# Performance work log

Hardware: AMD Instinct MI355X
Metric: run time of the kernel (lower is better)

## Reference

```python
import jax, jax.numpy as jnp
import numpy as np

# Irreps structure (hardcoded per init_kwargs):
#  input  = 16x0e + 8x1o  -> dim 16 + 8*3 = 40
#  query  = key = 8x0e + 4x1o -> dim 8 + 4*3 = 20
#  output = 16x0e + 8x1o -> dim 40
#  edge_sh = 1x0e + 1x1o -> dim 4
M0, M1 = 16, 8          # input multiplicities (scalar, vector)
Q0, Q1 = 8, 4           # query/key multiplicities
O0, O1 = 16, 8          # output multiplicities
TPK_NUMEL = M0*Q0 + M1*Q0 + M0*Q1 + M1*Q1 + M1*Q1   # 320
TPV_NUMEL = M0*O0 + M1*O0 + M0*O1 + M1*O1 + M1*O1   # 640
EDGE_BASIS = 16
HIDDEN = 32


def _split(x):
    """Split irreps vector [*, m0 + 3*m1] into scalars [*, m0] and vectors [*, m1, 3]."""
    m0 = x.shape[-1] - 3 * ((x.shape[-1] - M0) // 3) if False else None
    return x  # placeholder, not used


def fc_net(x, w1, w2):
    """e3nn FullyConnectedNet: no biases, 1/sqrt(fan_in) scaling, silu hidden act."""
    h = jax.nn.silu((x @ w1) * (1.0 / np.sqrt(x.shape[-1])))
    return (h @ w2) * (1.0 / np.sqrt(w1.shape[-1]))


def fctp_edge(xs, xv, shs, shv, w, o0, o1):
    """FullyConnectedTensorProduct((m0x0e+m1x1o) x (1x0e+1x1o) -> (o0x0e+o1x1o))
    with per-edge weights w [E, numel]. Component-normalized CG, path-normalized output.
    xs:[E,m0] xv:[E,m1,3] shs:[E,1] shv:[E,3]."""
    m0, m1 = xs.shape[1], xv.shape[1]
    sizes = [m0*o0, m1*o0, m0*o1, m1*o1, m1*o1]
    offs = np.cumsum([0] + sizes)
    w1 = w[:, offs[0]:offs[1]].reshape(-1, m0, o0)
    w2 = w[:, offs[1]:offs[2]].reshape(-1, m1, o0)
    w3 = w[:, offs[2]:offs[3]].reshape(-1, m0, o1)
    w4 = w[:, offs[3]:offs[4]].reshape(-1, m1, o1)
    w5 = w[:, offs[4]:offs[5]].reshape(-1, m1, o1)
    # scalar output paths: 0e x 0e -> 0e ; 1o x 1o -> 0e (dot / sqrt3)
    p_ss = xs * shs                                            # [E,m0]
    p_vv = jnp.einsum('eic,ec->ei', xv, shv) * (1.0/np.sqrt(3.0))  # [E,m1]
    out_s = (jnp.einsum('ei,eio->eo', p_ss, w1)
             + jnp.einsum('ei,eio->eo', p_vv, w2)) * (1.0/np.sqrt(m0 + m1))
    # vector output paths: 0e x 1o ; 1o x 0e ; 1o x 1o -> 1o (cross / sqrt2)
    p_sv = xs[:, :, None] * shv[:, None, :]                    # [E,m0,3]
    p_vs = xv * shs[:, :, None]                                # [E,m1,3]
    p_xx = jnp.cross(xv, shv[:, None, :]) * (1.0/np.sqrt(2.0)) # [E,m1,3]
    out_v = (jnp.einsum('eic,eio->eoc', p_sv, w3)
             + jnp.einsum('eic,eio->eoc', p_vs, w4)
             + jnp.einsum('eic,eio->eoc', p_xx, w5)) * (1.0/np.sqrt(m0 + 2*m1))
    return out_s, out_v


def setup_inputs() -> dict:
    key = jax.random.key(0)
    ks = jax.random.split(key, 12)
    N, E = 10000, 100000
    node_ft = jax.random.normal(ks[0], (N, M0 + 3*M1), dtype=jnp.float32)
    edge_index = jax.random.randint(ks[1], (2, E), 0, N, dtype=jnp.int64)
    edge_sh = jax.random.normal(ks[2], (E, 4), dtype=jnp.float32)
    edge_scalars = jax.random.uniform(ks[3], (E, EDGE_BASIS), dtype=jnp.float32)
    # learned parameters
    w_q_s = jax.random.normal(ks[4], (M0, Q0), dtype=jnp.float32)
    w_q_v = jax.random.normal(ks[5], (M1, Q1), dtype=jnp.float32)
    fck_w1 = jax.random.normal(ks[6], (EDGE_BASIS, HIDDEN), dtype=jnp.float32)
    fck_w2 = jax.random.normal(ks[7], (HIDDEN, TPK_NUMEL), dtype=jnp.float32)
    fcv_w1 = jax.random.normal(ks[8], (EDGE_BASIS, HIDDEN), dtype=jnp.float32)
    fcv_w2 = jax.random.normal(ks[9], (HIDDEN, TPV_NUMEL), dtype=jnp.float32)
    wdot_s = jax.random.normal(ks[10], (Q0, Q0), dtype=jnp.float32)
    wdot_v = jax.random.normal(ks[11], (Q1, Q1), dtype=jnp.float32)
    return dict(node_ft=node_ft, edge_index=edge_index, edge_sh=edge_sh,
                edge_scalars=edge_scalars, w_q_s=w_q_s, w_q_v=w_q_v,
                fck_w1=fck_w1, fck_w2=fck_w2, fcv_w1=fcv_w1, fcv_w2=fcv_w2,
                wdot_s=wdot_s, wdot_v=wdot_v)


def reference(node_ft, edge_index, edge_sh, edge_scalars, w_q_s, w_q_v,
              fck_w1, fck_w2, fcv_w1, fcv_w2, wdot_s, wdot_v):
    N = node_ft.shape[0]
    sender, receiver = edge_index[0], edge_index[1]
    x_s = node_ft[:, :M0]                       # [N,16]
    x_v = node_ft[:, M0:].reshape(N, M1, 3)     # [N,8,3]
    # q = o3.Linear(input -> query): per-irrep linear mixing, 1/sqrt(mul) norm
    q_s = (x_s @ w_q_s) * (1.0/np.sqrt(M0))                    # [N,Q0]
    q_v = jnp.einsum('nic,io->noc', x_v, w_q_v) * (1.0/np.sqrt(M1))  # [N,Q1,3]
    sh_s, sh_v = edge_sh[:, :1], edge_sh[:, 1:4]
    xs_e, xv_e = x_s[sender], x_v[sender]       # gather sender features
    # per-edge tensor-product weights from radial MLPs
    wk = fc_net(edge_scalars, fck_w1, fck_w2)   # [E, 320]
    wv = fc_net(edge_scalars, fcv_w1, fcv_w2)   # [E, 640]
    k_s, k_v = fctp_edge(xs_e, xv_e, sh_s, sh_v, wk, Q0, Q1)
    v_s, v_v = fctp_edge(xs_e, xv_e, sh_s, sh_v, wv, O0, O1)
    # dot = FCTP(query, key -> 0e) with shared internal weights
    qr_s, qr_v = q_s[receiver], q_v[receiver]
    fan = Q0*Q0 + Q1*Q1
    dot = (jnp.einsum('ei,ej,ij->e', qr_s, k_s, wdot_s)
           + jnp.einsum('eic,ejc,ij->e', qr_v, k_v, wdot_v) * (1.0/np.sqrt(3.0))
           ) * (1.0/np.sqrt(fan))               # [E]
    # scatter-softmax over receiver
    ex = jnp.exp(dot)
    z = jax.ops.segment_sum(ex, receiver, num_segments=N)      # [N]
    alpha = ex / z[receiver]
    a = jnp.sqrt(jax.nn.relu(alpha))            # [E]
    out_s = jax.ops.segment_sum(a[:, None] * v_s, receiver, num_segments=N)
    out_v = jax.ops.segment_sum(a[:, None, None] * v_v, receiver, num_segments=N)
    return jnp.concatenate([out_s, out_v.reshape(N, O1*3)], axis=-1)  # [N,40]
```

## Files before the change

### kernel.cpp

```cpp
#include <hip/hip_runtime.h>


#define BS 256
#define EPB 64

typedef _Float16 h2 __attribute__((ext_vector_type(2)));

__device__ __forceinline__ float silu_f(float x) {
    return x * (1.0f / (1.0f + __expf(-x)));
}
__device__ __forceinline__ unsigned short f2h(float f) {
    return __builtin_bit_cast(unsigned short, (_Float16)f);
}
__device__ __forceinline__ unsigned pk2h(float a, float b) {
    return (unsigned)f2h(a) | ((unsigned)f2h(b) << 16);
}
__device__ __forceinline__ h2 uh2(unsigned u) {
    return __builtin_bit_cast(h2, u);
}
__device__ __forceinline__ h2 pkrtz(float a, float b) {
    return __builtin_bit_cast(h2, __builtin_amdgcn_cvt_pkrtz(a, b));
}
__device__ __forceinline__ h2 pfma(h2 a, h2 b, h2 c) {
    return __builtin_elementwise_fma(a, b, c);
}
__device__ __forceinline__ float h2s(h2 a) {
    return (float)a[0] + (float)a[1];
}
__device__ __forceinline__ float wred4(float v) {
    v += __shfl_xor(v, 16);
    v += __shfl_xor(v, 32);
    return v;
}

__global__ __launch_bounds__(256) void node_pre(
    const float* __restrict__ node_ft,
    const int*   __restrict__ ei,
    const float* __restrict__ w_q_s, const float* __restrict__ w_q_v,
    const float* __restrict__ wdot_s, const float* __restrict__ wdot_v,
    float* __restrict__ qd, int* __restrict__ cnt, int* __restrict__ flag,
    int N, int E)
{
    const int n = blockIdx.x * blockDim.x + threadIdx.x;
    if (n == 0) {
        int acc = 0;
        const int kmax = (E < 64) ? E : 64;
        for (int k = 0; k < kmax; ++k) acc |= ei[2*k + 1];
        *flag = (acc == 0) ? 1 : 0;
    }
    if (n >= N) return;
    cnt[n] = 0;

    const float* nf = node_ft + (size_t)n * 40;
    float xs[16];
#pragma unroll
    for (int i = 0; i < 16; ++i) xs[i] = nf[i];
    float q[8];
#pragma unroll
    for (int o = 0; o < 8; ++o) {
        float a = 0.f;
#pragma unroll
        for (int i = 0; i < 16; ++i) a += xs[i] * w_q_s[i*8 + o];
        q[o] = a * 0.25f;
    }
    float* qdn = qd + (size_t)n * 20;
#pragma unroll
    for (int j = 0; j < 8; ++j) {
        float a = 0.f;
#pragma unroll
        for (int i = 0; i < 8; ++i) a += q[i] * wdot_s[i*8 + j];
        qdn[j] = a;
    }
    float xv[8][3];
#pragma unroll
    for (int i = 0; i < 8; ++i)
#pragma unroll
        for (int c = 0; c < 3; ++c) xv[i][c] = nf[16 + i*3 + c];
    float qv[4][3];
#pragma unroll
    for (int o = 0; o < 4; ++o)
#pragma unroll
        for (int c = 0; c < 3; ++c) {
            float a = 0.f;
#pragma unroll
            for (int i = 0; i < 8; ++i) a += xv[i][c] * w_q_v[i*4 + o];
            qv[o][c] = a * 0.35355339059327379f;
        }
#pragma unroll
    for (int j = 0; j < 4; ++j)
#pragma unroll
        for (int c = 0; c < 3; ++c) {
            float a = 0.f;
#pragma unroll
            for (int i = 0; i < 4; ++i) a += qv[i][c] * wdot_v[i*4 + j];
            qdn[8 + j*3 + c] = a;
        }
}

__global__ __launch_bounds__(256) void count_edges(
    const int* __restrict__ ei, int* __restrict__ cnt,
    const int* __restrict__ flag, int E)
{
    const int e = blockIdx.x * blockDim.x + threadIdx.x;
    if (e >= E) return;
    const int is64 = *flag;
    const int rcv = is64 ? ei[2*(E + e)] : ei[E + e];
    atomicAdd(cnt + rcv, 1);
}

__global__ __launch_bounds__(1024) void scan_kernel(
    const int* __restrict__ cnt, int* __restrict__ start,
    int* __restrict__ cursor, int N)
{
    __shared__ int wsum[16];
    __shared__ int s_carry;
    const int tid = threadIdx.x, wave = tid >> 6, lane = tid & 63;
    if (tid == 0) s_carry = 0;
    __syncthreads();
    for (int base = 0; base < N; base += 1024) {
        const int i = base + tid;
        const int v = (i < N) ? cnt[i] : 0;
        int x = v;
#pragma unroll
        for (int d = 1; d < 64; d <<= 1) {
            const int y = __shfl_up(x, d, 64);
            if (lane >= d) x += y;
        }
        if (lane == 63) wsum[wave] = x;
        __syncthreads();
        if (wave == 0 && lane < 16) {
            int w = wsum[lane];
#pragma unroll
            for (int d = 1; d < 16; d <<= 1) {
                const int y = __shfl_up(w, d, 64);
                if (lane >= d) w += y;
            }
            wsum[lane] = w;
        }
        __syncthreads();
        const int woff = (wave == 0) ? 0 : wsum[wave - 1];
        const int carry = s_carry;
        if (i < N) {
            const int s = carry + woff + x - v;
            start[i] = s;
            cursor[i] = s;
        }
        __syncthreads();
        if (tid == 0) s_carry = carry + wsum[15];
        __syncthreads();
    }
    if (tid == 0) start[N] = s_carry;
}

__global__ __launch_bounds__(BS) void edge_k(
    const float* __restrict__ node_ft,
    const int*   __restrict__ ei,
    const float* __restrict__ edge_sh,
    const float* __restrict__ edge_scalars,
    const float* __restrict__ fck_w1,
    const float* __restrict__ fck_w2,
    const float* __restrict__ qd,
    int*   __restrict__ cursor,
    float* __restrict__ exbuf,
    float* __restrict__ sabuf,
    int*   __restrict__ posbuf,
    const int* __restrict__ flag,
    int N, int E)
{
    __shared__ uint4 sk4[4 * 321];

    const int tid = threadIdx.x;
    for (int idx = tid; idx < 4 * 320; idx += BS) {
        const int p = idx / 320;
        const int local = idx - p * 320;
        unsigned r0, r1, r2, r3;
        if (local < 128) {
            const int j = local >> 2, rr = local & 3, ip = rr >> 1, h = rr & 1;
            const int i0 = 4*p + 2*ip;
            const float* s0 = fck_w2 + j*320 + i0*8 + 4*h;
            const float* s1 = s0 + 8;
            r0 = pk2h(s0[0], s1[0]); r1 = pk2h(s0[1], s1[1]);
            r2 = pk2h(s0[2], s1[2]); r3 = pk2h(s0[3], s1[3]);
        } else if (local < 192) {
            const int l = local - 128; const int j = l >> 1, ip = l & 1;
            const int i0 = 4*p + 2*ip;
            const float* s0 = fck_w2 + j*320 + 192 + i0*4;
            const float* s1 = s0 + 4;
            r0 = pk2h(s0[0], s1[0]); r1 = pk2h(s0[1], s1[1]);
            r2 = pk2h(s0[2], s1[2]); r3 = pk2h(s0[3], s1[3]);
        } else if (local < 256) {
            const int l = local - 192; const int j = l >> 1, h = l & 1;
            const int i0 = 2*p;
            const float* s0 = fck_w2 + j*320 + 128 + i0*8 + 4*h;
            const float* s1 = s0 + 8;
            r0 = pk2h(s0[0], s1[0]); r1 = pk2h(s0[1], s1[1]);
            r2 = pk2h(s0[2], s1[2]); r3 = pk2h(s0[3], s1[3]);
        } else {
            const int l = local - 256; const int jp = l >> 2, rr = l & 3;
            const int il = rr >> 1, h = rr & 1;
            const int i = 2*p + il, j0 = 2*jp;
            const int col = (h == 0 ? 256 : 288) + i*4;
            const float* s0 = fck_w2 + j0*320 + col;
            const float* s1 = s0 + 320;
            r0 = pk2h(s0[0], s1[0]); r1 = pk2h(s0[1], s1[1]);
            r2 = pk2h(s0[2], s1[2]); r3 = pk2h(s0[3], s1[3]);
        }
        sk4[p * 321 + local] = make_uint4(r0, r1, r2, r3);
    }

    const int lane = tid & 63;
    const int p = lane >> 4;
    const int q = lane & 15;
    const int w = tid >> 6;
    const int e = blockIdx.x * EPB + w * 16 + q;
    const bool val = (e < E);
    const int ec = val ? e : (E - 1);

    const int is64 = *flag;
    const int snd = is64 ? ei[2*ec]       : ei[ec];
    const int rcv = is64 ? ei[2*(E + ec)] : ei[E + ec];

    int pos = 0;
    if (p == 0 && val) pos = atomicAdd(cursor + rcv, 1);

    const float4 s4 = *(const float4*)(edge_sh + (size_t)ec * 4);
    const float sh_s = s4.x;
    const float sh_v[3] = {s4.y, s4.z, s4.w};

    const float* nf = node_ft + (size_t)snd * 40;

    __syncthreads();

    float hk[32];
    {
        float es[16];
        const float4* a0 = (const float4*)(edge_scalars + (size_t)ec * 16);
#pragma unroll
        for (int t = 0; t < 4; ++t) {
            const float4 v = a0[t];
            es[4*t+0]=v.x; es[4*t+1]=v.y; es[4*t+2]=v.z; es[4*t+3]=v.w;
        }
#pragma unroll 8
        for (int j = 0; j < 32; ++j) {
            float a = 0.f;
#pragma unroll
            for (int t = 0; t < 16; ++t) a += es[t] * fck_w1[t*32 + j];
            hk[j] = silu_f(a * 0.25f);
        }
    }

    const uint4* g = sk4 + p * 321;

    const h2 xs01 = pkrtz(nf[4*p + 0], nf[4*p + 1]);
    const h2 xs23 = pkrtz(nf[4*p + 2], nf[4*p + 3]);
    const float c3 = 0.57735026918962576f;
    const float x00 = nf[16 + 6*p], x01 = nf[17 + 6*p], x02 = nf[18 + 6*p];
    const float x10 = nf[19 + 6*p], x11 = nf[20 + 6*p], x12 = nf[21 + 6*p];
    const h2 pvp = pkrtz((x00*sh_v[0] + x01*sh_v[1] + x02*sh_v[2]) * c3,
                         (x10*sh_v[0] + x11*sh_v[1] + x12*sh_v[2]) * c3);

    h2 K1[8] = {}, K3[4] = {}, K2[8] = {};
#pragma unroll 4
    for (int j = 0; j < 32; ++j) {
        const uint4 A = g[j*4+0], B = g[j*4+1], C = g[j*4+2], D = g[j*4+3];
        const uint4 Ea = g[128 + j*2], Fb = g[128 + j*2 + 1];
        const uint4 U = g[192 + j*2], V = g[192 + j*2 + 1];
        const h2 hh = pkrtz(hk[j], hk[j]);
        const h2 t01 = hh * xs01, t23 = hh * xs23, tp = hh * pvp;
        K1[0]=pfma(t01,uh2(A.x),K1[0]); K1[0]=pfma(t23,uh2(C.x),K1[0]);
        K1[1]=pfma(t01,uh2(A.y),K1[1]); K1[1]=pfma(t23,uh2(C.y),K1[1]);
        K1[2]=pfma(t01,uh2(A.z),K1[2]); K1[2]=pfma(t23,uh2(C.z),K1[2]);
        K1[3]=pfma(t01,uh2(A.w),K1[3]); K1[3]=pfma(t23,uh2(C.w),K1[3]);
        K1[4]=pfma(t01,uh2(B.x),K1[4]); K1[4]=pfma(t23,uh2(D.x),K1[4]);
        K1[5]=pfma(t01,uh2(B.y),K1[5]); K1[5]=pfma(t23,uh2(D.y),K1[5]);
        K1[6]=pfma(t01,uh2(B.z),K1[6]); K1[6]=pfma(t23,uh2(D.z),K1[6]);
        K1[7]=pfma(t01,uh2(B.w),K1[7]); K1[7]=pfma(t23,uh2(D.w),K1[7]);
        K3[0]=pfma(t01,uh2(Ea.x),K3[0]); K3[0]=pfma(t23,uh2(Fb.x),K3[0]);
        K3[1]=pfma(t01,uh2(Ea.y),K3[1]); K3[1]=pfma(t23,uh2(Fb.y),K3[1]);
        K3[2]=pfma(t01,uh2(Ea.z),K3[2]); K3[2]=pfma(t23,uh2(Fb.z),K3[2]);
        K3[3]=pfma(t01,uh2(Ea.w),K3[3]); K3[3]=pfma(t23,uh2(Fb.w),K3[3]);
        K2[0]=pfma(tp,uh2(U.x),K2[0]); K2[1]=pfma(tp,uh2(U.y),K2[1]);
        K2[2]=pfma(tp,uh2(U.z),K2[2]); K2[3]=pfma(tp,uh2(U.w),K2[3]);
        K2[4]=pfma(tp,uh2(V.x),K2[4]); K2[5]=pfma(tp,uh2(V.y),K2[5]);
        K2[6]=pfma(tp,uh2(V.z),K2[6]); K2[7]=pfma(tp,uh2(V.w),K2[7]);
    }

    h2 P4[8] = {}, P5[8] = {};
#pragma unroll 4
    for (int jp = 0; jp < 16; ++jp) {
        const uint4 a4 = g[256 + jp*4 + 0];
        const uint4 b4 = g[256 + jp*4 + 1];
        const uint4 c4 = g[256 + jp*4 + 2];
        const uint4 d4 = g[256 + jp*4 + 3];
        const h2 hp = pkrtz(hk[2*jp], hk[2*jp+1]);
        P4[0]=pfma(hp,uh2(a4.x),P4[0]); P4[1]=pfma(hp,uh2(a4.y),P4[1]);
        P4[2]=pfma(hp,uh2(a4.z),P4[2]); P4[3]=pfma(hp,uh2(a4.w),P4[3]);
        P5[0]=pfma(hp,uh2(b4.x),P5[0]); P5[1]=pfma(hp,uh2(b4.y),P5[1]);
        P5[2]=pfma(hp,uh2(b4.z),P5[2]); P5[3]=pfma(hp,uh2(b4.w),P5[3]);
        P4[4]=pfma(hp,uh2(c4.x),P4[4]); P4[5]=pfma(hp,uh2(c4.y),P4[5]);
        P4[6]=pfma(hp,uh2(c4.z),P4[6]); P4[7]=pfma(hp,uh2(c4.w),P4[7]);
        P5[4]=pfma(hp,uh2(d4.x),P5[4]); P5[5]=pfma(hp,uh2(d4.y),P5[5]);
        P5[6]=pfma(hp,uh2(d4.z),P5[6]); P5[7]=pfma(hp,uh2(d4.w),P5[7]);
    }

    const float c7 = 0.70710678118654752f;
    float ds = 0.f, dv = 0.f;
    {
        float qdr[20];
        const float4* rp = (const float4*)(qd + (size_t)rcv * 20);
#pragma unroll
        for (int t = 0; t < 5; ++t) {
            const float4 a = rp[t];
            qdr[4*t+0]=a.x; qdr[4*t+1]=a.y; qdr[4*t+2]=a.z; qdr[4*t+3]=a.w;
        }
#pragma unroll
        for (int o = 0; o < 8; ++o)
            ds += qdr[o] * (sh_s*h2s(K1[o]) + h2s(K2[o]));
        float KV[12] = {};
        {
            const float s0=sh_s*x00, s1=sh_s*x01, s2=sh_s*x02;
            const float cx0=c7*(x01*sh_v[2]-x02*sh_v[1]);
            const float cx1=c7*(x02*sh_v[0]-x00*sh_v[2]);
            const float cx2=c7*(x00*sh_v[1]-x01*sh_v[0]);
#pragma unroll
            for (int o = 0; o < 4; ++o) {
                const float w4 = h2s(P4[o]), w5 = h2s(P5[o]);
                KV[o*3+0] += s0*w4 + cx0*w5;
                KV[o*3+1] += s1*w4 + cx1*w5;
                KV[o*3+2] += s2*w4 + cx2*w5;
            }
        }
        {
            const float s0=sh_s*x10, s1=sh_s*x11, s2=sh_s*x12;
            const float cx0=c7*(x11*sh_v[2]-x12*sh_v[1]);
            const float cx1=c7*(x12*sh_v[0]-x10*sh_v[2]);
            const float cx2=c7*(x10*sh_v[1]-x11*sh_v[0]);
#pragma unroll
            for (int o = 0; o < 4; ++o) {
                const float w4 = h2s(P4[4+o]), w5 = h2s(P5[4+o]);
                KV[o*3+0] += s0*w4 + cx0*w5;
                KV[o*3+1] += s1*w4 + cx1*w5;
                KV[o*3+2] += s2*w4 + cx2*w5;
            }
        }
#pragma unroll
        for (int o = 0; o < 4; ++o) {
            const float k3 = h2s(K3[o]);
#pragma unroll
            for (int c = 0; c < 3; ++c)
                dv += qdr[8 + o*3 + c] * (k3*sh_v[c] + KV[o*3+c]);
        }
    }
    ds = wred4(ds); dv = wred4(dv);

    if (p == 0 && val) {
        const float dot = ds * 4.0343567508008e-3f + dv * 2.0171788261497e-3f;
        const float sa = __expf(0.5f * dot);
        exbuf[pos] = sa*sa; sabuf[e] = sa; posbuf[e] = pos;
    }
}

__global__ __launch_bounds__(BS) void edge_v_a(
    const float* __restrict__ node_ft,
    const int*   __restrict__ ei,
    const float* __restrict__ edge_sh,
    const float* __restrict__ edge_scalars,
    const float* __restrict__ fcv_w1,
    const float* __restrict__ fcv_w2,
    const float* __restrict__ sabuf,
    const int*   __restrict__ posbuf,
    float* __restrict__ vbuf,
    const int* __restrict__ flag,
    int E)
{
    __shared__ uint4 sa4[4 * 385];

    const int tid = threadIdx.x;
    for (int idx = tid; idx < 4 * 384; idx += BS) {
        const int p = idx / 384;
        const int local = idx - p * 384;
        const float* s0;
        const float* s1;
        if (local < 256) {
            const int j = local >> 3, rr = local & 7, ip = rr >> 2, h = rr & 3;
            const int i0 = 4*p + 2*ip;
            s0 = fcv_w2 + j*640 + i0*16 + h*4;
            s1 = s0 + 16;
        } else {
            const int l = local - 256; const int j = l >> 2, h = l & 3;
            const int i0 = 2*p;
            s0 = fcv_w2 + j*640 + 256 + i0*16 + h*4;
            s1 = s0 + 16;
        }
        sa4[p * 385 + local] = make_uint4(
            pk2h(s0[0], s1[0]), pk2h(s0[1], s1[1]),
            pk2h(s0[2], s1[2]), pk2h(s0[3], s1[3]));
    }

    const int lane = tid & 63;
    const int p = lane >> 4;
    const int q = lane & 15;
    const int w = tid >> 6;
    const int e = blockIdx.x * EPB + w * 16 + q;
    const bool val = (e < E);
    const int ec = val ? e : (E - 1);

    const int is64 = *flag;
    const int snd = is64 ? ei[2*ec] : ei[ec];

    const float4 s4 = *(const float4*)(edge_sh + (size_t)ec * 4);

    const float* nf = node_ft + (size_t)snd * 40;

    __syncthreads();

    float hv[32];
    {
        float es[16];
        const float4* a0 = (const float4*)(edge_scalars + (size_t)ec * 16);
#pragma unroll
        for (int t = 0; t < 4; ++t) {
            const float4 v = a0[t];
            es[4*t+0]=v.x; es[4*t+1]=v.y; es[4*t+2]=v.z; es[4*t+3]=v.w;
        }
#pragma unroll 8
        for (int j = 0; j < 32; ++j) {
            float a = 0.f;
#pragma unroll
            for (int t = 0; t < 16; ++t) a += es[t] * fcv_w1[t*32 + j];
            hv[j] = silu_f(a * 0.25f);
        }
    }

    const uint4* g = sa4 + p * 385;

    const h2 xs01 = pkrtz(nf[4*p + 0]*s4.x, nf[4*p + 1]*s4.x);
    const h2 xs23 = pkrtz(nf[4*p + 2]*s4.x, nf[4*p + 3]*s4.x);
    const float c3 = 0.57735026918962576f;
    const h2 pvp = pkrtz(
        (nf[16+6*p]*s4.y + nf[17+6*p]*s4.z + nf[18+6*p]*s4.w) * c3,
        (nf[19+6*p]*s4.y + nf[20+6*p]*s4.z + nf[21+6*p]*s4.w) * c3);

    h2 Aa[16] = {};
#pragma unroll 4
    for (int j = 0; j < 32; ++j) {
        const uint4* gw = g + j*8;
        const uint4 a0 = gw[0], a1 = gw[1], a2 = gw[2], a3 = gw[3];
        const uint4 b0 = gw[4], b1 = gw[5], b2 = gw[6], b3 = gw[7];
        const uint4* g2 = g + 256 + j*4;
        const uint4 u0 = g2[0], u1 = g2[1], u2 = g2[2], u3 = g2[3];
        const h2 hh = pkrtz(hv[j], hv[j]);
        const h2 t01 = hh * xs01, t23 = hh * xs23, tp = hh * pvp;
        Aa[0] =pfma(t01,uh2(a0.x),Aa[0]);  Aa[0] =pfma(t23,uh2(b0.x),Aa[0]);  Aa[0] =pfma(tp,uh2(u0.x),Aa[0]);
        Aa[1] =pfma(t01,uh2(a0.y),Aa[1]);  Aa[1] =pfma(t23,uh2(b0.y),Aa[1]);  Aa[1] =pfma(tp,uh2(u0.y),Aa[1]);
        Aa[2] =pfma(t01,uh2(a0.z),Aa[2]);  Aa[2] =pfma(t23,uh2(b0.z),Aa[2]);  Aa[2] =pfma(tp,uh2(u0.z),Aa[2]);
        Aa[3] =pfma(t01,uh2(a0.w),Aa[3]);  Aa[3] =pfma(t23,uh2(b0.w),Aa[3]);  Aa[3] =pfma(tp,uh2(u0.w),Aa[3]);
        Aa[4] =pfma(t01,uh2(a1.x),Aa[4]);  Aa[4] =pfma(t23,uh2(b1.x),Aa[4]);  Aa[4] =pfma(tp,uh2(u1.x),Aa[4]);
        Aa[5] =pfma(t01,uh2(a1.y),Aa[5]);  Aa[5] =pfma(t23,uh2(b1.y),Aa[5]);  Aa[5] =pfma(tp,uh2(u1.y),Aa[5]);
        Aa[6] =pfma(t01,uh2(a1.z),Aa[6]);  Aa[6] =pfma(t23,uh2(b1.z),Aa[6]);  Aa[6] =pfma(tp,uh2(u1.z),Aa[6]);
        Aa[7] =pfma(t01,uh2(a1.w),Aa[7]);  Aa[7] =pfma(t23,uh2(b1.w),Aa[7]);  Aa[7] =pfma(tp,uh2(u1.w),Aa[7]);
        Aa[8] =pfma(t01,uh2(a2.x),Aa[8]);  Aa[8] =pfma(t23,uh2(b2.x),Aa[8]);  Aa[8] =pfma(tp,uh2(u2.x),Aa[8]);
        Aa[9] =pfma(t01,uh2(a2.y),Aa[9]);  Aa[9] =pfma(t23,uh2(b2.y),Aa[9]);  Aa[9] =pfma(tp,uh2(u2.y),Aa[9]);
        Aa[10]=pfma(t01,uh2(a2.z),Aa[10]); Aa[10]=pfma(t23,uh2(b2.z),Aa[10]); Aa[10]=pfma(tp,uh2(u2.z),Aa[10]);
        Aa[11]=pfma(t01,uh2(a2.w),Aa[11]); Aa[11]=pfma(t23,uh2(b2.w),Aa[11]); Aa[11]=pfma(tp,uh2(u2.w),Aa[11]);
        Aa[12]=pfma(t01,uh2(a3.x),Aa[12]); Aa[12]=pfma(t23,uh2(b3.x),Aa[12]); Aa[12]=pfma(tp,uh2(u3.x),Aa[12]);
        Aa[13]=pfma(t01,uh2(a3.y),Aa[13]); Aa[13]=pfma(t23,uh2(b3.y),Aa[13]); Aa[13]=pfma(tp,uh2(u3.y),Aa[13]);
        Aa[14]=pfma(t01,uh2(a3.z),Aa[14]); Aa[14]=pfma(t23,uh2(b3.z),Aa[14]); Aa[14]=pfma(tp,uh2(u3.z),Aa[14]);
        Aa[15]=pfma(t01,uh2(a3.w),Aa[15]); Aa[15]=pfma(t23,uh2(b3.w),Aa[15]); Aa[15]=pfma(tp,uh2(u3.w),Aa[15]);
    }

    float A0[16];
#pragma unroll
    for (int o = 0; o < 16; ++o) A0[o] = wred4(h2s(Aa[o]));

    if (p == 0 && val) {
        const float cs = 0.03608439182435161f;
        const float sa = sabuf[e];
        const int pos = posbuf[e];
        float4* vp = (float4*)(vbuf + (size_t)pos * 40);
#pragma unroll
        for (int t = 0; t < 4; ++t) {
            float4 r;
            r.x = sa * A0[4*t+0] * cs; r.y = sa * A0[4*t+1] * cs;
            r.z = sa * A0[4*t+2] * cs; r.w = sa * A0[4*t+3] * cs;
            vp[t] = r;
        }
    }
}

__global__ __launch_bounds__(BS) void edge_v_b(
    const float* __restrict__ node_ft,
    const int*   __restrict__ ei,
    const float* __restrict__ edge_sh,
    const float* __restrict__ edge_scalars,
    const float* __restrict__ fcv_w1,
    const float* __restrict__ fcv_w2,
    const float* __restrict__ sabuf,
    const int*   __restrict__ posbuf,
    float* __restrict__ vbuf,
    const int* __restrict__ flag,
    int E)
{
    __shared__ uint4 sb4[4 * 257];

    const int tid = threadIdx.x;
    for (int idx = tid; idx < 4 * 256; idx += BS) {
        const int p = idx >> 8;
        const int local = idx & 255;
        const float* s0;
        const float* s1;
        if (local < 128) {
            const int j = local >> 2, rr = local & 3, ip = rr >> 1, h = rr & 1;
            const int i0 = 4*p + 2*ip;
            s0 = fcv_w2 + j*640 + 384 + i0*8 + 4*h;
            s1 = s0 + 8;
        } else {
            const int l = local - 128;
            const int jp = l >> 3, rr = l & 7, il = rr >> 2, h2c = rr & 3;
            const int i = 2*p + il, j0 = 2*jp;
            const int base = (h2c < 2) ? 512 : 576;
            s0 = fcv_w2 + j0*640 + base + i*8 + (h2c & 1)*4;
            s1 = s0 + 640;
        }
        sb4[p * 257 + local] = make_uint4(
            pk2h(s0[0], s1[0]), pk2h(s0[1], s1[1]),
            pk2h(s0[2], s1[2]), pk2h(s0[3], s1[3]));
    }

    const int lane = tid & 63;
    const int p = lane >> 4;
    const int q = lane & 15;
    const int w = tid >> 6;
    const int e = blockIdx.x * EPB + w * 16 + q;
    const bool val = (e < E);
    const int ec = val ? e : (E - 1);

    const int is64 = *flag;
    const int snd = is64 ? ei[2*ec] : ei[ec];

    const float4 s4 = *(const float4*)(edge_sh + (size_t)ec * 4);
    const float sh_s = s4.x;
    const float sh_v[3] = {s4.y, s4.z, s4.w};

    const float* nf = node_ft + (size_t)snd * 40;

    __syncthreads();

    float hv[32];
    {
        float es[16];
        const float4* a0 = (const float4*)(edge_scalars + (size_t)ec * 16);
#pragma unroll
        for (int t = 0; t < 4; ++t) {
            const float4 v = a0[t];
            es[4*t+0]=v.x; es[4*t+1]=v.y; es[4*t+2]=v.z; es[4*t+3]=v.w;
        }
#pragma unroll 8
        for (int j = 0; j < 32; ++j) {
            float a = 0.f;
#pragma unroll
            for (int t = 0; t < 16; ++t) a += es[t] * fcv_w1[t*32 + j];
            hv[j] = silu_f(a * 0.25f);
        }
    }

    const uint4* g = sb4 + p * 257;

    const h2 xs01 = pkrtz(nf[4*p + 0], nf[4*p + 1]);
    const h2 xs23 = pkrtz(nf[4*p + 2], nf[4*p + 3]);

    h2 T3[8] = {};
#pragma unroll 4
    for (int j = 0; j < 32; ++j) {
        const uint4 E0 = g[j*4+0], E1 = g[j*4+1];
        const uint4 F0 = g[j*4+2], F1 = g[j*4+3];
        const h2 hh = pkrtz(hv[j], hv[j]);
        const h2 t01 = hh * xs01, t23 = hh * xs23;
        T3[0]=pfma(t01,uh2(E0.x),T3[0]); T3[0]=pfma(t23,uh2(F0.x),T3[0]);
        T3[1]=pfma(t01,uh2(E0.y),T3[1]); T3[1]=pfma(t23,uh2(F0.y),T3[1]);
        T3[2]=pfma(t01,uh2(E0.z),T3[2]); T3[2]=pfma(t23,uh2(F0.z),T3[2]);
        T3[3]=pfma(t01,uh2(E0.w),T3[3]); T3[3]=pfma(t23,uh2(F0.w),T3[3]);
        T3[4]=pfma(t01,uh2(E1.x),T3[4]); T3[4]=pfma(t23,uh2(F1.x),T3[4]);
        T3[5]=pfma(t01,uh2(E1.y),T3[5]); T3[5]=pfma(t23,uh2(F1.y),T3[5]);
        T3[6]=pfma(t01,uh2(E1.z),T3[6]); T3[6]=pfma(t23,uh2(F1.z),T3[6]);
        T3[7]=pfma(t01,uh2(E1.w),T3[7]); T3[7]=pfma(t23,uh2(F1.w),T3[7]);
    }

    h2 P4[16] = {}, P5[16] = {};
#pragma unroll 2
    for (int jp = 0; jp < 16; ++jp) {
        const uint4* gw = g + 128 + jp*8;
        const uint4 a4 = gw[0], b4 = gw[1];
        const uint4 c4 = gw[2], d4 = gw[3];
        const uint4 e4 = gw[4], f4 = gw[5];
        const uint4 m4 = gw[6], n4 = gw[7];
        const h2 hp = pkrtz(hv[2*jp], hv[2*jp+1]);
        P4[0] =pfma(hp,uh2(a4.x),P4[0]);  P4[1] =pfma(hp,uh2(a4.y),P4[1]);
        P4[2] =pfma(hp,uh2(a4.z),P4[2]);  P4[3] =pfma(hp,uh2(a4.w),P4[3]);
        P4[4] =pfma(hp,uh2(b4.x),P4[4]);  P4[5] =pfma(hp,uh2(b4.y),P4[5]);
        P4[6] =pfma(hp,uh2(b4.z),P4[6]);  P4[7] =pfma(hp,uh2(b4.w),P4[7]);
        P5[0] =pfma(hp,uh2(c4.x),P5[0]);  P5[1] =pfma(hp,uh2(c4.y),P5[1]);
        P5[2] =pfma(hp,uh2(c4.z),P5[2]);  P5[3] =pfma(hp,uh2(c4.w),P5[3]);
        P5[4] =pfma(hp,uh2(d4.x),P5[4]);  P5[5] =pfma(hp,uh2(d4.y),P5[5]);
        P5[6] =pfma(hp,uh2(d4.z),P5[6]);  P5[7] =pfma(hp,uh2(d4.w),P5[7]);
        P4[8] =pfma(hp,uh2(e4.x),P4[8]);  P4[9] =pfma(hp,uh2(e4.y),P4[9]);
        P4[10]=pfma(hp,uh2(e4.z),P4[10]); P4[11]=pfma(hp,uh2(e4.w),P4[11]);
        P4[12]=pfma(hp,uh2(f4.x),P4[12]); P4[13]=pfma(hp,uh2(f4.y),P4[13]);
        P4[14]=pfma(hp,uh2(f4.z),P4[14]); P4[15]=pfma(hp,uh2(f4.w),P4[15]);
        P5[8] =pfma(hp,uh2(m4.x),P5[8]);  P5[9] =pfma(hp,uh2(m4.y),P5[9]);
        P5[10]=pfma(hp,uh2(m4.z),P5[10]); P5[11]=pfma(hp,uh2(m4.w),P5[11]);
        P5[12]=pfma(hp,uh2(n4.x),P5[12]); P5[13]=pfma(hp,uh2(n4.y),P5[13]);
        P5[14]=pfma(hp,uh2(n4.z),P5[14]); P5[15]=pfma(hp,uh2(n4.w),P5[15]);
    }

    const float c7 = 0.70710678118654752f;
    float R[24], T3f[8];
    {
        float acc[24];
#pragma unroll
        for (int o = 0; o < 24; ++o) acc[o] = 0.f;
        {
            const float x0 = nf[16 + 6*p], x1 = nf[17 + 6*p], x2 = nf[18 + 6*p];
            const float s0 = sh_s*x0, s1 = sh_s*x1, s2 = sh_s*x2;
            const float cx0 = c7*(x1*sh_v[2] - x2*sh_v[1]);
            const float cx1 = c7*(x2*sh_v[0] - x0*sh_v[2]);
            const float cx2 = c7*(x0*sh_v[1] - x1*sh_v[0]);
#pragma unroll
            for (int o = 0; o < 8; ++o) {
                const float w4 = h2s(P4[o]), w5 = h2s(P5[o]);
                acc[o*3+0] += s0*w4 + cx0*w5;
                acc[o*3+1] += s1*w4 + cx1*w5;
                acc[o*3+2] += s2*w4 + cx2*w5;
            }
        }
        {
            const float x0 = nf[19 + 6*p], x1 = nf[20 + 6*p], x2 = nf[21 + 6*p];
            const float s0 = sh_s*x0, s1 = sh_s*x1, s2 = sh_s*x2;
            const float cx0 = c7*(x1*sh_v[2] - x2*sh_v[1]);
            const float cx1 = c7*(x2*sh_v[0] - x0*sh_v[2]);
            const float cx2 = c7*(x0*sh_v[1] - x1*sh_v[0]);
#pragma unroll
            for (int o = 0; o < 8; ++o) {
                const float w4 = h2s(P4[8+o]), w5 = h2s(P5[8+o]);
                acc[o*3+0] += s0*w4 + cx0*w5;
                acc[o*3+1] += s1*w4 + cx1*w5;
                acc[o*3+2] += s2*w4 + cx2*w5;
            }
        }
#pragma unroll
        for (int o = 0; o < 24; ++o) R[o] = wred4(acc[o]);
    }
#pragma unroll
    for (int o = 0; o < 8; ++o) T3f[o] = wred4(h2s(T3[o]));

    if (p == 0 && val) {
        const float sc = 0.03125f;
        const float sa = sabuf[e];
        const int pos = posbuf[e];
        float row[24];
#pragma unroll
        for (int o = 0; o < 8; ++o)
#pragma unroll
            for (int c = 0; c < 3; ++c)
                row[o*3+c] = sa * (T3f[o]*sh_v[c] + R[o*3+c]) * sc;
        float4* vp = (float4*)(vbuf + (size_t)pos * 40 + 16);
#pragma unroll
        for (int t = 0; t < 6; ++t) {
            float4 r; r.x = row[4*t+0]; r.y = row[4*t+1]; r.z = row[4*t+2]; r.w = row[4*t+3];
            vp[t] = r;
        }
    }
}

__global__ __launch_bounds__(256) void node_reduce(
    const int*   __restrict__ start,
    const float* __restrict__ exbuf,
    const float* __restrict__ vbuf,
    float* __restrict__ out, int N)
{
    const int wave = threadIdx.x >> 6;
    const int lane = threadIdx.x & 63;
    const int n = blockIdx.x * 4 + wave;
    if (n >= N) return;
    const int r0 = start[n], r1 = start[n + 1];
    float z = 0.f, comp = 0.f;
    for (int r = r0; r < r1; ++r) {
        z += exbuf[r];
        if (lane < 40) comp += vbuf[(size_t)r * 40 + lane];
    }
    if (lane < 40)
        out[(size_t)n * 40 + lane] = (z > 0.f) ? comp * rsqrtf(z) : 0.f;
}

extern "C" void kernel_launch(void* const* d_in, const int* in_sizes, int n_in,
                              void* d_out, int out_size, void* d_ws, size_t ws_size,
                              hipStream_t stream) {
    const float* node_ft      = (const float*)d_in[0];
    const int*   edge_index   = (const int*)  d_in[1];
    const float* edge_sh      = (const float*)d_in[2];
    const float* edge_scalars = (const float*)d_in[3];
    const float* w_q_s        = (const float*)d_in[4];
    const float* w_q_v        = (const float*)d_in[5];
    const float* fck_w1       = (const float*)d_in[6];
    const float* fck_w2       = (const float*)d_in[7];
    const float* fcv_w1       = (const float*)d_in[8];
    const float* fcv_w2       = (const float*)d_in[9];
    const float* wdot_s       = (const float*)d_in[10];
    const float* wdot_v       = (const float*)d_in[11];

    const int N = in_sizes[0] / 40;
    const int E = in_sizes[2] / 4;

    float* ws    = (float*)d_ws;
    float* qd    = ws;
    int*   cnt   = (int*)(ws + (size_t)N * 20);
    int*   start = cnt + N;
    int*   curs  = start + N + 1;
    int*   flg   = curs + N;
    size_t off   = (size_t)N * 20 + N + (N + 1) + N + 1;
    off = (off + 3) & ~(size_t)3;
    float* exbuf  = ws + off;
    float* sabuf  = exbuf + E;
    int*   posbuf = (int*)(sabuf + E);
    float* vbuf   = (float*)(posbuf + E);

    float* out = (float*)d_out;

    const int EB = (E + EPB - 1) / EPB;

    hipLaunchKernelGGL(node_pre, dim3((N + 255) / 256), dim3(256), 0, stream,
                       node_ft, edge_index, w_q_s, w_q_v, wdot_s, wdot_v,
                       qd, cnt, flg, N, E);
    hipLaunchKernelGGL(count_edges, dim3((E + 255) / 256), dim3(256), 0, stream,
                       edge_index, cnt, flg, E);
    hipLaunchKernelGGL(scan_kernel, dim3(1), dim3(1024), 0, stream,
                       cnt, start, curs, N);
    hipLaunchKernelGGL(edge_k, dim3(EB), dim3(BS), 0, stream,
                       node_ft, edge_index, edge_sh, edge_scalars,
                       fck_w1, fck_w2, qd, curs, exbuf, sabuf, posbuf, flg, N, E);
    hipLaunchKernelGGL(edge_v_a, dim3(EB), dim3(BS), 0, stream,
                       node_ft, edge_index, edge_sh, edge_scalars,
                       fcv_w1, fcv_w2, sabuf, posbuf, vbuf, flg, E);
    hipLaunchKernelGGL(edge_v_b, dim3(EB), dim3(BS), 0, stream,
                       node_ft, edge_index, edge_sh, edge_scalars,
                       fcv_w1, fcv_w2, sabuf, posbuf, vbuf, flg, E);
    hipLaunchKernelGGL(node_reduce, dim3((N + 3) / 4), dim3(256), 0, stream,
                       start, exbuf, vbuf, out, N);
}
```

Baseline: 269.2 us.

## Fuse edge key and value kernels into one pass, merge node prep with edge counting

The separate key/dot kernel and the two value kernels become a single edge kernel. It computes the attention score and the value tensor product in one pass and writes the value rows directly. This drops the intermediate sabuf/posbuf round trips, two kernel launches, and the repeated gathers of node features, edge scalars and indices. Node query preparation and edge counting are merged into one launch, with a memset zeroing the counts. The cost is a larger shared-memory swizzle buffer and more live registers per thread, which may reduce occupancy.

```diff
diff --git a/kernel.cpp b/kernel.cpp
--- a/kernel.cpp
+++ b/kernel.cpp
@@ -33,7 +33,7 @@
     return v;
 }
 
-__global__ __launch_bounds__(256) void node_pre(
+__global__ __launch_bounds__(256) void pre_count(
     const float* __restrict__ node_ft,
     const int*   __restrict__ ei,
     const float* __restrict__ w_q_s, const float* __restrict__ w_q_v,
@@ -41,34 +41,43 @@
     float* __restrict__ qd, int* __restrict__ cnt, int* __restrict__ flag,
     int N, int E)
 {
-    const int n = blockIdx.x * blockDim.x + threadIdx.x;
-    if (n == 0) {
-        int acc = 0;
+    const int gid = blockIdx.x * blockDim.x + threadIdx.x;
+
+    int acc = 0;
+    if ((threadIdx.x & 63) == 0) {
         const int kmax = (E < 64) ? E : 64;
         for (int k = 0; k < kmax; ++k) acc |= ei[2*k + 1];
-        *flag = (acc == 0) ? 1 : 0;
-    }
+    }
+    acc = __shfl(acc, 0, 64);
+    const int is64 = (acc == 0) ? 1 : 0;
+    if (gid == 0) *flag = is64;
+
+    if (gid < E) {
+        const int rcv = is64 ? ei[2*(E + gid)] : ei[E + gid];
+        atomicAdd(cnt + rcv, 1);
+    }
+
+    const int n = gid;
     if (n >= N) return;
-    cnt[n] = 0;
 
     const float* nf = node_ft + (size_t)n * 40;
     float xs[16];
 #pragma unroll
     for (int i = 0; i < 16; ++i) xs[i] = nf[i];
-    float q[8];
+    float qv0[8];
 #pragma unroll
     for (int o = 0; o < 8; ++o) {
         float a = 0.f;
 #pragma unroll
         for (int i = 0; i < 16; ++i) a += xs[i] * w_q_s[i*8 + o];
-        q[o] = a * 0.25f;
+        qv0[o] = a * 0.25f;
     }
     float* qdn = qd + (size_t)n * 20;
 #pragma unroll
     for (int j = 0; j < 8; ++j) {
         float a = 0.f;
 #pragma unroll
-        for (int i = 0; i < 8; ++i) a += q[i] * wdot_s[i*8 + j];
+        for (int i = 0; i < 8; ++i) a += qv0[i] * wdot_s[i*8 + j];
         qdn[j] = a;
     }
     float xv[8][3];
@@ -95,17 +104,6 @@
             for (int i = 0; i < 4; ++i) a += qv[i][c] * wdot_v[i*4 + j];
             qdn[8 + j*3 + c] = a;
         }
-}
-
-__global__ __launch_bounds__(256) void count_edges(
-    const int* __restrict__ ei, int* __restrict__ cnt,
-    const int* __restrict__ flag, int E)
-{
-    const int e = blockIdx.x * blockDim.x + threadIdx.x;
-    if (e >= E) return;
-    const int is64 = *flag;
-    const int rcv = is64 ? ei[2*(E + e)] : ei[E + e];
-    atomicAdd(cnt + rcv, 1);
 }
 
 __global__ __launch_bounds__(1024) void scan_kernel(
@@ -152,45 +150,78 @@
     if (tid == 0) start[N] = s_carry;
 }
 
-__global__ __launch_bounds__(BS) void edge_k(
+__global__ __launch_bounds__(BS) void edge_all(
     const float* __restrict__ node_ft,
     const int*   __restrict__ ei,
     const float* __restrict__ edge_sh,
     const float* __restrict__ edge_scalars,
     const float* __restrict__ fck_w1,
     const float* __restrict__ fck_w2,
+    const float* __restrict__ fcv_w1,
+    const float* __restrict__ fcv_w2,
     const float* __restrict__ qd,
     int*   __restrict__ cursor,
     float* __restrict__ exbuf,
-    float* __restrict__ sabuf,
-    int*   __restrict__ posbuf,
+    float* __restrict__ vbuf,
     const int* __restrict__ flag,
     int N, int E)
 {
-    __shared__ uint4 sk4[4 * 321];
+    __shared__ uint4 swz[4 * 385];
 
     const int tid = threadIdx.x;
+    const int lane = tid & 63;
+    const int p = lane >> 4;
+    const int q = lane & 15;
+    const int w = tid >> 6;
+    const int e = blockIdx.x * EPB + w * 16 + q;
+    const bool val = (e < E);
+    const int ec = val ? e : (E - 1);
+
+    const int is64 = *flag;
+    const int snd = is64 ? ei[2*ec]       : ei[ec];
+    const int rcv = is64 ? ei[2*(E + ec)] : ei[E + ec];
+
+    int pos = 0;
+    if (p == 0 && val) pos = atomicAdd(cursor + rcv, 1);
+
+    const float4 s4 = *(const float4*)(edge_sh + (size_t)ec * 4);
+    const float sh_s = s4.x;
+    const float sh_v[3] = {s4.y, s4.z, s4.w};
+    const float* nf = node_ft + (size_t)snd * 40;
+    const float c3 = 0.57735026918962576f;
+    const float c7 = 0.70710678118654752f;
+
+    float es[16];
+    {
+        const float4* a0 = (const float4*)(edge_scalars + (size_t)ec * 16);
+#pragma unroll
+        for (int t = 0; t < 4; ++t) {
+            const float4 v = a0[t];
+            es[4*t+0]=v.x; es[4*t+1]=v.y; es[4*t+2]=v.z; es[4*t+3]=v.w;
+        }
+    }
+
     for (int idx = tid; idx < 4 * 320; idx += BS) {
-        const int p = idx / 320;
-        const int local = idx - p * 320;
+        const int pg = idx / 320;
+        const int local = idx - pg * 320;
         unsigned r0, r1, r2, r3;
         if (local < 128) {
             const int j = local >> 2, rr = local & 3, ip = rr >> 1, h = rr & 1;
-            const int i0 = 4*p + 2*ip;
+            const int i0 = 4*pg + 2*ip;
             const float* s0 = fck_w2 + j*320 + i0*8 + 4*h;
             const float* s1 = s0 + 8;
             r0 = pk2h(s0[0], s1[0]); r1 = pk2h(s0[1], s1[1]);
             r2 = pk2h(s0[2], s1[2]); r3 = pk2h(s0[3], s1[3]);
         } else if (local < 192) {
             const int l = local - 128; const int j = l >> 1, ip = l & 1;
-            const int i0 = 4*p + 2*ip;
+            const int i0 = 4*pg + 2*ip;
             const float* s0 = fck_w2 + j*320 + 192 + i0*4;
             const float* s1 = s0 + 4;
             r0 = pk2h(s0[0], s1[0]); r1 = pk2h(s0[1], s1[1]);
             r2 = pk2h(s0[2], s1[2]); r3 = pk2h(s0[3], s1[3]);
         } else if (local < 256) {
             const int l = local - 192; const int j = l >> 1, h = l & 1;
-            const int i0 = 2*p;
+            const int i0 = 2*pg;
             const float* s0 = fck_w2 + j*320 + 128 + i0*8 + 4*h;
             const float* s1 = s0 + 8;
             r0 = pk2h(s0[0], s1[0]); r1 = pk2h(s0[1], s1[1]);
@@ -198,48 +229,20 @@
         } else {
             const int l = local - 256; const int jp = l >> 2, rr = l & 3;
             const int il = rr >> 1, h = rr & 1;
-            const int i = 2*p + il, j0 = 2*jp;
+            const int i = 2*pg + il, j0 = 2*jp;
             const int col = (h == 0 ? 256 : 288) + i*4;
             const float* s0 = fck_w2 + j0*320 + col;
             const float* s1 = s0 + 320;
             r0 = pk2h(s0[0], s1[0]); r1 = pk2h(s0[1], s1[1]);
             r2 = pk2h(s0[2], s1[2]); r3 = pk2h(s0[3], s1[3]);
         }
-        sk4[p * 321 + local] = make_uint4(r0, r1, r2, r3);
-    }
-
-    const int lane = tid & 63;
-    const int p = lane >> 4;
-    const int q = lane & 15;
-    const int w = tid >> 6;
-    const int e = blockIdx.x * EPB + w * 16 + q;
-    const bool val = (e < E);
-    const int ec = val ? e : (E - 1);
-
-    const int is64 = *flag;
-    const int snd = is64 ? ei[2*ec]       : ei[ec];
-    const int rcv = is64 ? ei[2*(E + ec)] : ei[E + ec];
-
-    int pos = 0;
-    if (p == 0 && val) pos = atomicAdd(cursor + rcv, 1);
-
-    const float4 s4 = *(const float4*)(edge_sh + (size_t)ec * 4);
-    const float sh_s = s4.x;
-    const float sh_v[3] = {s4.y, s4.z, s4.w};
-
-    const float* nf = node_ft + (size_t)snd * 40;
-
+        swz[pg * 321 + local] = make_uint4(r0, r1, r2, r3);
+    }
     __syncthreads();
 
-    float hk[32];
+    float sa = 0.f;
     {
-        float es[16];
-        const float4* a0 = (const float4*)(edge_scalars + (size_t)ec * 16);
-#pragma unroll
-        for (int t = 0; t < 4; ++t) {
-            const float4 v = a0[t];
-            es[4*t+0]=v.x; es[4*t+1]=v.y; es[4*t+2]=v.z; es[4*t+3]=v.w;
-        }
+        float hk[32];
 #pragma unroll 8
         for (int j = 0; j < 32; ++j) {
             float a = 0.f;
@@ -247,427 +250,330 @@
             for (int t = 0; t < 16; ++t) a += es[t] * fck_w1[t*32 + j];
             hk[j] = silu_f(a * 0.25f);
         }
-    }
-
-    const uint4* g = sk4 + p * 321;
-
-    const h2 xs01 = pkrtz(nf[4*p + 0], nf[4*p + 1]);
-    const h2 xs23 = pkrtz(nf[4*p + 2], nf[4*p + 3]);
-    const float c3 = 0.57735026918962576f;
-    const float x00 = nf[16 + 6*p], x01 = nf[17 + 6*p], x02 = nf[18 + 6*p];
-    const float x10 = nf[19 + 6*p], x11 = nf[20 + 6*p], x12 = nf[21 + 6*p];
-    const h2 pvp = pkrtz((x00*sh_v[0] + x01*sh_v[1] + x02*sh_v[2]) * c3,
-                         (x10*sh_v[0] + x11*sh_v[1] + x12*sh_v[2]) * c3);
-
-    h2 K1[8] = {}, K3[4] = {}, K2[8] = {};
+
+        const uint4* g = swz + p * 321;
+
+        const h2 xs01 = pkrtz(nf[4*p + 0], nf[4*p + 1]);
+        const h2 xs23 = pkrtz(nf[4*p + 2], nf[4*p + 3]);
+        const float x00 = nf[16 + 6*p], x01 = nf[17 + 6*p], x02 = nf[18 + 6*p];
+        const float x10 = nf[19 + 6*p], x11 = nf[20 + 6*p], x12 = nf[21 + 6*p];
+        const h2 pvp = pkrtz((x00*sh_v[0] + x01*sh_v[1] + x02*sh_v[2]) * c3,
+                             (x10*sh_v[0] + x11*sh_v[1] + x12*sh_v[2]) * c3);
+
+        h2 K1[8] = {}, K3[4] = {}, K2[8] = {};
 #pragma unroll 4
-    for (int j = 0; j < 32; ++j) {
-        const uint4 A = g[j*4+0], B = g[j*4+1], C = g[j*4+2], D = g[j*4+3];
-        const uint4 Ea = g[128 + j*2], Fb = g[128 + j*2 + 1];
-        const uint4 U = g[192 + j*2], V = g[192 + j*2 + 1];
-        const h2 hh = pkrtz(hk[j], hk[j]);
-        const h2 t01 = hh * xs01, t23 = hh * xs23, tp = hh * pvp;
-        K1[0]=pfma(t01,uh2(A.x),K1[0]); K1[0]=pfma(t23,uh2(C.x),K1[0]);
-        K1[1]=pfma(t01,uh2(A.y),K1[1]); K1[1]=pfma(t23,uh2(C.y),K1[1]);
-        K1[2]=pfma(t01,uh2(A.z),K1[2]); K1[2]=pfma(t23,uh2(C.z),K1[2]);
-        K1[3]=pfma(t01,uh2(A.w),K1[3]); K1[3]=pfma(t23,uh2(C.w),K1[3]);
-        K1[4]=pfma(t01,uh2(B.x),K1[4]); K1[4]=pfma(t23,uh2(D.x),K1[4]);
-        K1[5]=pfma(t01,uh2(B.y),K1[5]); K1[5]=pfma(t23,uh2(D.y),K1[5]);
-        K1[6]=pfma(t01,uh2(B.z),K1[6]); K1[6]=pfma(t23,uh2(D.z),K1[6]);
-        K1[7]=pfma(t01,uh2(B.w),K1[7]); K1[7]=pfma(t23,uh2(D.w),K1[7]);
-        K3[0]=pfma(t01,uh2(Ea.x),K3[0]); K3[0]=pfma(t23,uh2(Fb.x),K3[0]);
-        K3[1]=pfma(t01,uh2(Ea.y),K3[1]); K3[1]=pfma(t23,uh2(Fb.y),K3[1]);
-        K3[2]=pfma(t01,uh2(Ea.z),K3[2]); K3[2]=pfma(t23,uh2(Fb.z),K3[2]);
-        K3[3]=pfma(t01,uh2(Ea.w),K3[3]); K3[3]=pfma(t23,uh2(Fb.w),K3[3]);
-        K2[0]=pfma(tp,uh2(U.x),K2[0]); K2[1]=pfma(tp,uh2(U.y),K2[1]);
-        K2[2]=pfma(tp,uh2(U.z),K2[2]); K2[3]=pfma(tp,uh2(U.w),K2[3]);
-        K2[4]=pfma(tp,uh2(V.x),K2[4]); K2[5]=pfma(tp,uh2(V.y),K2[5]);
-        K2[6]=pfma(tp,uh2(V.z),K2[6]); K2[7]=pfma(tp,uh2(V.w),K2[7]);
-    }
-
-    h2 P4[8] = {}, P5[8] = {};
+        for (int j = 0; j < 32; ++j) {
+            const uint4 A = g[j*4+0], B = g[j*4+1], C = g[j*4+2], D = g[j*4+3];
+            const uint4 Ea = g[128 + j*2], Fb = g[128 + j*2 + 1];
+            const uint4 U = g[192 + j*2], V = g[192 + j*2 + 1];
+            const h2 hh = pkrtz(hk[j], hk[j]);
+            const h2 t01 = hh * xs01, t23 = hh * xs23, tp = hh * pvp;
+            K1[0]=pfma(t01,uh2(A.x),K1[0]); K1[0]=pfma(t23,uh2(C.x),K1[0]);
+            K1[1]=pfma(t01,uh2(A.y),K1[1]); K1[1]=pfma(t23,uh2(C.y),K1[1]);
+            K1[2]=pfma(t01,uh2(A.z),K1[2]); K1[2]=pfma(t23,uh2(C.z),K1[2]);
+            K1[3]=pfma(t01,uh2(A.w),K1[3]); K1[3]=pfma(t23,uh2(C.w),K1[3]);
+            K1[4]=pfma(t01,uh2(B.x),K1[4]); K1[4]=pfma(t23,uh2(D.x),K1[4]);
+            K1[5]=pfma(t01,uh2(B.y),K1[5]); K1[5]=pfma(t23,uh2(D.y),K1[5]);
+            K1[6]=pfma(t01,uh2(B.z),K1[6]); K1[6]=pfma(t23,uh2(D.z),K1[6]);
+            K1[7]=pfma(t01,uh2(B.w),K1[7]); K1[7]=pfma(t23,uh2(D.w),K1[7]);
+            K3[0]=pfma(t01,uh2(Ea.x),K3[0]); K3[0]=pfma(t23,uh2(Fb.x),K3[0]);
+            K3[1]=pfma(t01,uh2(Ea.y),K3[1]); K3[1]=pfma(t23,uh2(Fb.y),K3[1]);
+            K3[2]=pfma(t01,uh2(Ea.z),K3[2]); K3[2]=pfma(t23,uh2(Fb.z),K3[2]);
+            K3[3]=pfma(t01,uh2(Ea.w),K3[3]); K3[3]=pfma(t23,uh2(Fb.w),K3[3]);
+            K2[0]=pfma(tp,uh2(U.x),K2[0]); K2[1]=pfma(tp,uh2(U.y),K2[1]);
+            K2[2]=pfma(tp,uh2(U.z),K2[2]); K2[3]=pfma(tp,uh2(U.w),K2[3]);
+            K2[4]=pfma(tp,uh2(V.x),K2[4]); K2[5]=pfma(tp,uh2(V.y),K2[5]);
+            K2[6]=pfma(tp,uh2(V.z),K2[6]); K2[7]=pfma(tp,uh2(V.w),K2[7]);
+        }
+
+        h2 P4[8] = {}, P5[8] = {};
 #pragma unroll 4
-    for (int jp = 0; jp < 16; ++jp) {
-        const uint4 a4 = g[256 + jp*4 + 0];
-        const uint4 b4 = g[256 + jp*4 + 1];
-        const uint4 c4 = g[256 + jp*4 + 2];
-        const uint4 d4 = g[256 + jp*4 + 3];
-        const h2 hp = pkrtz(hk[2*jp], hk[2*jp+1]);
-        P4[0]=pfma(hp,uh2(a4.x),P4[0]); P4[1]=pfma(hp,uh2(a4.y),P4[1]);
-        P4[2]=pfma(hp,uh2(a4.z),P4[2]); P4[3]=pfma(hp,uh2(a4.w),P4[3]);
-        P5[0]=pfma(hp,uh2(b4.x),P5[0]); P5[1]=pfma(hp,uh2(b4.y),P5[1]);
-        P5[2]=pfma(hp,uh2(b4.z),P5[2]); P5[3]=pfma(hp,uh2(b4.w),P5[3]);
-        P4[4]=pfma(hp,uh2(c4.x),P4[4]); P4[5]=pfma(hp,uh2(c4.y),P4[5]);
-        P4[6]=pfma(hp,uh2(c4.z),P4[6]); P4[7]=pfma(hp,uh2(c4.w),P4[7]);
-        P5[4]=pfma(hp,uh2(d4.x),P5[4]); P5[5]=pfma(hp,uh2(d4.y),P5[5]);
-        P5[6]=pfma(hp,uh2(d4.z),P5[6]); P5[7]=pfma(hp,uh2(d4.w),P5[7]);
-    }
-
-    const float c7 = 0.70710678118654752f;
-    float ds = 0.f, dv = 0.f;
-    {
-        float qdr[20];
-        const float4* rp = (const float4*)(qd + (size_t)rcv * 20);
-#pragma unroll
-        for (int t = 0; t < 5; ++t) {
-            const float4 a = rp[t];
-            qdr[4*t+0]=a.x; qdr[4*t+1]=a.y; qdr[4*t+2]=a.z; qdr[4*t+3]=a.w;
-        }
-#pragma unroll
-        for (int o = 0; o < 8; ++o)
-            ds += qdr[o] * (sh_s*h2s(K1[o]) + h2s(K2[o]));
-        float KV[12] = {};
+        for (int jp = 0; jp < 16; ++jp) {
+            const uint4 a4 = g[256 + jp*4 + 0];
+            const uint4 b4 = g[256 + jp*4 + 1];
+            const uint4 c4 = g[256 + jp*4 + 2];
+            const uint4 d4 = g[256 + jp*4 + 3];
+            const h2 hp = pkrtz(hk[2*jp], hk[2*jp+1]);
+            P4[0]=pfma(hp,uh2(a4.x),P4[0]); P4[1]=pfma(hp,uh2(a4.y),P4[1]);
+            P4[2]=pfma(hp,uh2(a4.z),P4[2]); P4[3]=pfma(hp,uh2(a4.w),P4[3]);
+            P5[0]=pfma(hp,uh2(b4.x),P5[0]); P5[1]=pfma(hp,uh2(b4.y),P5[1]);
+            P5[2]=pfma(hp,uh2(b4.z),P5[2]); P5[3]=pfma(hp,uh2(b4.w),P5[3]);
+            P4[4]=pfma(hp,uh2(c4.x),P4[4]); P4[5]=pfma(hp,uh2(c4.y),P4[5]);
+            P4[6]=pfma(hp,uh2(c4.z),P4[6]); P4[7]=pfma(hp,uh2(c4.w),P4[7]);
+            P5[4]=pfma(hp,uh2(d4.x),P5[4]); P5[5]=pfma(hp,uh2(d4.y),P5[5]);
+            P5[6]=pfma(hp,uh2(d4.z),P5[6]); P5[7]=pfma(hp,uh2(d4.w),P5[7]);
+        }
+
+        float ds = 0.f, dv = 0.f;
         {
-            const float s0=sh_s*x00, s1=sh_s*x01, s2=sh_s*x02;
-            const float cx0=c7*(x01*sh_v[2]-x02*sh_v[1]);
-            const float cx1=c7*(x02*sh_v[0]-x00*sh_v[2]);
-            const float cx2=c7*(x00*sh_v[1]-x01*sh_v[0]);
+            float qdr[20];
+            const float4* rp = (const float4*)(qd + (size_t)rcv * 20);
+#pragma unroll
+            for (int t = 0; t < 5; ++t) {
+                const float4 a = rp[t];
+                qdr[4*t+0]=a.x; qdr[4*t+1]=a.y; qdr[4*t+2]=a.z; qdr[4*t+3]=a.w;
+            }
+#pragma unroll
+            for (int o = 0; o < 8; ++o)
+                ds += qdr[o] * (sh_s*h2s(K1[o]) + h2s(K2[o]));
+            float KV[12] = {};
+            {
+                const float s0=sh_s*x00, s1=sh_s*x01, s2=sh_s*x02;
+                const float cx0=c7*(x01*sh_v[2]-x02*sh_v[1]);
+                const float cx1=c7*(x02*sh_v[0]-x00*sh_v[2]);
+                const float cx2=c7*(x00*sh_v[1]-x01*sh_v[0]);
+#pragma unroll
+                for (int o = 0; o < 4; ++o) {
+                    const float w4 = h2s(P4[o]), w5 = h2s(P5[o]);
+                    KV[o*3+0] += s0*w4 + cx0*w5;
+                    KV[o*3+1] += s1*w4 + cx1*w5;
+                    KV[o*3+2] += s2*w4 + cx2*w5;
+                }
+            }
+            {
+                const float s0=sh_s*x10, s1=sh_s*x11, s2=sh_s*x12;
+                const float cx0=c7*(x11*sh_v[2]-x12*sh_v[1]);
+                const float cx1=c7*(x12*sh_v[0]-x10*sh_v[2]);
+                const float cx2=c7*(x10*sh_v[1]-x11*sh_v[0]);
+#pragma unroll
+                for (int o = 0; o < 4; ++o) {
+                    const float w4 = h2s(P4[4+o]), w5 = h2s(P5[4+o]);
+                    KV[o*3+0] += s0*w4 + cx0*w5;
+                    KV[o*3+1] += s1*w4 + cx1*w5;
+                    KV[o*3+2] += s2*w4 + cx2*w5;
+                }
+            }
 #pragma unroll
             for (int o = 0; o < 4; ++o) {
-                const float w4 = h2s(P4[o]), w5 = h2s(P5[o]);
-                KV[o*3+0] += s0*w4 + cx0*w5;
-                KV[o*3+1] += s1*w4 + cx1*w5;
-                KV[o*3+2] += s2*w4 + cx2*w5;
-            }
-        }
-        {
-            const float s0=sh_s*x10, s1=sh_s*x11, s2=sh_s*x12;
-            const float cx0=c7*(x11*sh_v[2]-x12*sh_v[1]);
-            const float cx1=c7*(x12*sh_v[0]-x10*sh_v[2]);
-            const float cx2=c7*(x10*sh_v[1]-x11*sh_v[0]);
-#pragma unroll
-            for (int o = 0; o < 4; ++o) {
-                const float w4 = h2s(P4[4+o]), w5 = h2s(P5[4+o]);
-                KV[o*3+0] += s0*w4 + cx0*w5;
-                KV[o*3+1] += s1*w4 + cx1*w5;
-                KV[o*3+2] += s2*w4 + cx2*w5;
-            }
-        }
-#pragma unroll
-        for (int o = 0; o < 4; ++o) {
-            const float k3 = h2s(K3[o]);
-#pragma unroll
-            for (int c = 0; c < 3; ++c)
-                dv += qdr[8 + o*3 + c] * (k3*sh_v[c] + KV[o*3+c]);
-        }
-    }
-    ds = wred4(ds); dv = wred4(dv);
-
-    if (p == 0 && val) {
-        const float dot = ds * 4.0343567508008e-3f + dv * 2.0171788261497e-3f;
-        const float sa = __expf(0.5f * dot);
-        exbuf[pos] = sa*sa; sabuf[e] = sa; posbuf[e] = pos;
-    }
-}
-
-__global__ __launch_bounds__(BS) void edge_v_a(
-    const float* __restrict__ node_ft,
-    const int*   __restrict__ ei,
-    const float* __restrict__ edge_sh,
-    const float* __restrict__ edge_scalars,
-    const float* __restrict__ fcv_w1,
-    const float* __restrict__ fcv_w2,
-    const float* __restrict__ sabuf,
-    const int*   __restrict__ posbuf,
-    float* __restrict__ vbuf,
-    const int* __restrict__ flag,
-    int E)
-{
-    __shared__ uint4 sa4[4 * 385];
-
-    const int tid = threadIdx.x;
+                const float k3 = h2s(K3[o]);
+#pragma unroll
+                for (int c = 0; c < 3; ++c)
+                    dv += qdr[8 + o*3 + c] * (k3*sh_v[c] + KV[o*3+c]);
+            }
+        }
+        ds = wred4(ds); dv = wred4(dv);
+
+        if (p == 0 && val) {
+            const float dot = ds * 4.0343567508008e-3f + dv * 2.0171788261497e-3f;
+            sa = __expf(0.5f * dot);
+            exbuf[pos] = sa * sa;
+        }
+    }
+
+    __syncthreads();
     for (int idx = tid; idx < 4 * 384; idx += BS) {
-        const int p = idx / 384;
-        const int local = idx - p * 384;
+        const int pg = idx / 384;
+        const int local = idx - pg * 384;
         const float* s0;
         const float* s1;
         if (local < 256) {
             const int j = local >> 3, rr = local & 7, ip = rr >> 2, h = rr & 3;
-            const int i0 = 4*p + 2*ip;
+            const int i0 = 4*pg + 2*ip;
             s0 = fcv_w2 + j*640 + i0*16 + h*4;
             s1 = s0 + 16;
         } else {
             const int l = local - 256; const int j = l >> 2, h = l & 3;
-            const int i0 = 2*p;
+            const int i0 = 2*pg;
             s0 = fcv_w2 + j*640 + 256 + i0*16 + h*4;
             s1 = s0 + 16;
         }
-        sa4[p * 385 + local] = make_uint4(
+        swz[pg * 385 + local] = make_uint4(
             pk2h(s0[0], s1[0]), pk2h(s0[1], s1[1]),
             pk2h(s0[2], s1[2]), pk2h(s0[3], s1[3]));
     }
-
-    const int lane = tid & 63;
-    const int p = lane >> 4;
-    const int q = lane & 15;
-    const int w = tid >> 6;
-    const int e = blockIdx.x * EPB + w * 16 + q;
-    const bool val = (e < E);
-    const int ec = val ? e : (E - 1);
-
-    const int is64 = *flag;
-    const int snd = is64 ? ei[2*ec] : ei[ec];
-
-    const float4 s4 = *(const float4*)(edge_sh + (size_t)ec * 4);
-
-    const float* nf = node_ft + (size_t)snd * 40;
-
     __syncthreads();
 
     float hv[32];
+#pragma unroll 8
+    for (int j = 0; j < 32; ++j) {
+        float a = 0.f;
+#pragma unroll
+        for (int t = 0; t < 16; ++t) a += es[t] * fcv_w1[t*32 + j];
+        hv[j] = silu_f(a * 0.25f);
+    }
+
     {
-        float es[16];
-        const float4* a0 = (const float4*)(edge_scalars + (size_t)ec * 16);
-#pragma unroll
-        for (int t = 0; t < 4; ++t) {
-            const float4 v = a0[t];
-            es[4*t+0]=v.x; es[4*t+1]=v.y; es[4*t+2]=v.z; es[4*t+3]=v.w;
-        }
-#pragma unroll 8
+        const uint4* g = swz + p * 385;
+
+        const h2 xs01 = pkrtz(nf[4*p + 0]*sh_s, nf[4*p + 1]*sh_s);
+        const h2 xs23 = pkrtz(nf[4*p + 2]*sh_s, nf[4*p + 3]*sh_s);
+        const h2 pvp = pkrtz(
+            (nf[16+6*p]*sh_v[0] + nf[17+6*p]*sh_v[1] + nf[18+6*p]*sh_v[2]) * c3,
+            (nf[19+6*p]*sh_v[0] + nf[20+6*p]*sh_v[1] + nf[21+6*p]*sh_v[2]) * c3);
+
+        h2 Aa[16] = {};
+#pragma unroll 4
         for (int j = 0; j < 32; ++j) {
-            float a = 0.f;
-#pragma unroll
-            for (int t = 0; t < 16; ++t) a += es[t] * fcv_w1[t*32 + j];
-            hv[j] = silu_f(a * 0.25f);
-        }
-    }
-
-    const uint4* g = sa4 + p * 385;
-
-    const h2 xs01 = pkrtz(nf[4*p + 0]*s4.x, nf[4*p + 1]*s4.x);
-    const h2 xs23 = pkrtz(nf[4*p + 2]*s4.x, nf[4*p + 3]*s4.x);
-    const float c3 = 0.57735026918962576f;
-    const h2 pvp = pkrtz(
-        (nf[16+6*p]*s4.y + nf[17+6*p]*s4.z + nf[18+6*p]*s4.w) * c3,
-        (nf[19+6*p]*s4.y + nf[20+6*p]*s4.z + nf[21+6*p]*s4.w) * c3);
-
-    h2 Aa[16] = {};
-#pragma unroll 4
-    for (int j = 0; j < 32; ++j) {
-        const uint4* gw = g + j*8;
-        const uint4 a0 = gw[0], a1 = gw[1], a2 = gw[2], a3 = gw[3];
-        const uint4 b0 = gw[4], b1 = gw[5], b2 = gw[6], b3 = gw[7];
-        const uint4* g2 = g + 256 + j*4;
-        const uint4 u0 = g2[0], u1 = g2[1], u2 = g2[2], u3 = g2[3];
-        const h2 hh = pkrtz(hv[j], hv[j]);
-        const h2 t01 = hh * xs01, t23 = hh * xs23, tp = hh * pvp;
-        Aa[0] =pfma(t01,uh2(a0.x),Aa[0]);  Aa[0] =pfma(t23,uh2(b0.x),Aa[0]);  Aa[0] =pfma(tp,uh2(u0.x),Aa[0]);
-        Aa[1] =pfma(t01,uh2(a0.y),Aa[1]);  Aa[1] =pfma(t23,uh2(b0.y),Aa[1]);  Aa[1] =pfma(tp,uh2(u0.y),Aa[1]);
-        Aa[2] =pfma(t01,uh2(a0.z),Aa[2]);  Aa[2] =pfma(t23,uh2(b0.z),Aa[2]);  Aa[2] =pfma(tp,uh2(u0.z),Aa[2]);
-        Aa[3] =pfma(t01,uh2(a0.w),Aa[3]);  Aa[3] =pfma(t23,uh2(b0.w),Aa[3]);  Aa[3] =pfma(tp,uh2(u0.w),Aa[3]);
-        Aa[4] =pfma(t01,uh2(a1.x),Aa[4]);  Aa[4] =pfma(t23,uh2(b1.x),Aa[4]);  Aa[4] =pfma(tp,uh2(u1.x),Aa[4]);
-        Aa[5] =pfma(t01,uh2(a1.y),Aa[5]);  Aa[5] =pfma(t23,uh2(b1.y),Aa[5]);  Aa[5] =pfma(tp,uh2(u1.y),Aa[5]);
-        Aa[6] =pfma(t01,uh2(a1.z),Aa[6]);  Aa[6] =pfma(t23,uh2(b1.z),Aa[6]);  Aa[6] =pfma(tp,uh2(u1.z),Aa[6]);
-        Aa[7] =pfma(t01,uh2(a1.w),Aa[7]);  Aa[7] =pfma(t23,uh2(b1.w),Aa[7]);  Aa[7] =pfma(tp,uh2(u1.w),Aa[7]);
-        Aa[8] =pfma(t01,uh2(a2.x),Aa[8]);  Aa[8] =pfma(t23,uh2(b2.x),Aa[8]);  Aa[8] =pfma(tp,uh2(u2.x),Aa[8]);
-        Aa[9] =pfma(t01,uh2(a2.y),Aa[9]);  Aa[9] =pfma(t23,uh2(b2.y),Aa[9]);  Aa[9] =pfma(tp,uh2(u2.y),Aa[9]);
-        Aa[10]=pfma(t01,uh2(a2.z),Aa[10]); Aa[10]=pfma(t23,uh2(b2.z),Aa[10]); Aa[10]=pfma(tp,uh2(u2.z),Aa[10]);
-        Aa[11]=pfma(t01,uh2(a2.w),Aa[11]); Aa[11]=pfma(t23,uh2(b2.w),Aa[11]); Aa[11]=pfma(tp,uh2(u2.w),Aa[11]);
-        Aa[12]=pfma(t01,uh2(a3.x),Aa[12]); Aa[12]=pfma(t23,uh2(b3.x),Aa[12]); Aa[12]=pfma(tp,uh2(u3.x),Aa[12]);
-        Aa[13]=pfma(t01,uh2(a3.y),Aa[13]); Aa[13]=pfma(t23,uh2(b3.y),Aa[13]); Aa[13]=pfma(tp,uh2(u3.y),Aa[13]);
-        Aa[14]=pfma(t01,uh2(a3.z),Aa[14]); Aa[14]=pfma(t23,uh2(b3.z),Aa[14]); Aa[14]=pfma(tp,uh2(u3.z),Aa[14]);
-        Aa[15]=pfma(t01,uh2(a3.w),Aa[15]); Aa[15]=pfma(t23,uh2(b3.w),Aa[15]); Aa[15]=pfma(tp,uh2(u3.w),Aa[15]);
-    }
-
-    float A0[16];
-#pragma unroll
-    for (int o = 0; o < 16; ++o) A0[o] = wred4(h2s(Aa[o]));
-
-    if (p == 0 && val) {
-        const float cs = 0.03608439182435161f;
-        const float sa = sabuf[e];
-        const int pos = posbuf[e];
-        float4* vp = (float4*)(vbuf + (size_t)pos * 40);
-#pragma unroll
-        for (int t = 0; t < 4; ++t) {
-            float4 r;
-            r.x = sa * A0[4*t+0] * cs; r.y = sa * A0[4*t+1] * cs;
-            r.z = sa * A0[4*t+2] * cs; r.w = sa * A0[4*t+3] * cs;
-            vp[t] = r;
-        }
-    }
-}
-
-__global__ __launch_bounds__(BS) void edge_v_b(
-    const float* __restrict__ node_ft,
-    const int*   __restrict__ ei,
-    const float* __restrict__ edge_sh,
-    const float* __restrict__ edge_scalars,
-    const float* __restrict__ fcv_w1,
-    const float* __restrict__ fcv_w2,
-    const float* __restrict__ sabuf,
-    const int*   __restrict__ posbuf,
-    float* __restrict__ vbuf,
-    const int* __restrict__ flag,
-    int E)
-{
-    __shared__ uint4 sb4[4 * 257];
-
-    const int tid = threadIdx.x;
+            const uint4* gw = g + j*8;
+            const uint4 a0 = gw[0], a1 = gw[1], a2 = gw[2], a3 = gw[3];
+            const uint4 b0 = gw[4], b1 = gw[5], b2 = gw[6], b3 = gw[7];
+            const uint4* g2 = g + 256 + j*4;
+            const uint4 u0 = g2[0], u1 = g2[1], u2 = g2[2], u3 = g2[3];
+            const h2 hh = pkrtz(hv[j], hv[j]);
+            const h2 t01 = hh * xs01, t23 = hh * xs23, tp = hh * pvp;
+            Aa[0] =pfma(t01,uh2(a0.x),Aa[0]);  Aa[0] =pfma(t23,uh2(b0.x),Aa[0]);  Aa[0] =pfma(tp,uh2(u0.x),Aa[0]);
+            Aa[1] =pfma(t01,uh2(a0.y),Aa[1]);  Aa[1] =pfma(t23,uh2(b0.y),Aa[1]);  Aa[1] =pfma(tp,uh2(u0.y),Aa[1]);
+            Aa[2] =pfma(t01,uh2(a0.z),Aa[2]);  Aa[2] =pfma(t23,uh2(b0.z),Aa[2]);  Aa[2] =pfma(tp,uh2(u0.z),Aa[2]);
+            Aa[3] =pfma(t01,uh2(a0.w),Aa[3]);  Aa[3] =pfma(t23,uh2(b0.w),Aa[3]);  Aa[3] =pfma(tp,uh2(u0.w),Aa[3]);
+            Aa[4] =pfma(t01,uh2(a1.x),Aa[4]);  Aa[4] =pfma(t23,uh2(b1.x),Aa[4]);  Aa[4] =pfma(tp,uh2(u1.x),Aa[4]);
+            Aa[5] =pfma(t01,uh2(a1.y),Aa[5]);  Aa[5] =pfma(t23,uh2(b1.y),Aa[5]);  Aa[5] =pfma(tp,uh2(u1.y),Aa[5]);
+            Aa[6] =pfma(t01,uh2(a1.z),Aa[6]);  Aa[6] =pfma(t23,uh2(b1.z),Aa[6]);  Aa[6] =pfma(tp,uh2(u1.z),Aa[6]);
+            Aa[7] =pfma(t01,uh2(a1.w),Aa[7]);  Aa[7] =pfma(t23,uh2(b1.w),Aa[7]);  Aa[7] =pfma(tp,uh2(u1.w),Aa[7]);
+            Aa[8] =pfma(t01,uh2(a2.x),Aa[8]);  Aa[8] =pfma(t23,uh2(b2.x),Aa[8]);  Aa[8] =pfma(tp,uh2(u2.x),Aa[8]);
+            Aa[9] =pfma(t01,uh2(a2.y),Aa[9]);  Aa[9] =pfma(t23,uh2(b2.y),Aa[9]);  Aa[9] =pfma(tp,uh2(u2.y),Aa[9]);
+            Aa[10]=pfma(t01,uh2(a2.z),Aa[10]); Aa[10]=pfma(t23,uh2(b2.z),Aa[10]); Aa[10]=pfma(tp,uh2(u2.z),Aa[10]);
+            Aa[11]=pfma(t01,uh2(a2.w),Aa[11]); Aa[11]=pfma(t23,uh2(b2.w),Aa[11]); Aa[11]=pfma(tp,uh2(u2.w),Aa[11]);
+            Aa[12]=pfma(t01,uh2(a3.x),Aa[12]); Aa[12]=pfma(t23,uh2(b3.x),Aa[12]); Aa[12]=pfma(tp,uh2(u3.x),Aa[12]);
+            Aa[13]=pfma(t01,uh2(a3.y),Aa[13]); Aa[13]=pfma(t23,uh2(b3.y),Aa[13]); Aa[13]=pfma(tp,uh2(u3.y),Aa[13]);
+            Aa[14]=pfma(t01,uh2(a3.z),Aa[14]); Aa[14]=pfma(t23,uh2(b3.z),Aa[14]); Aa[14]=pfma(tp,uh2(u3.z),Aa[14]);
+            Aa[15]=pfma(t01,uh2(a3.w),Aa[15]); Aa[15]=pfma(t23,uh2(b3.w),Aa[15]); Aa[15]=pfma(tp,uh2(u3.w),Aa[15]);
+        }
+
+        float A0[16];
+#pragma unroll
+        for (int o = 0; o < 16; ++o) A0[o] = wred4(h2s(Aa[o]));
+
+        if (p == 0 && val) {
+            const float cs = 0.03608439182435161f;
+            float4* vp = (float4*)(vbuf + (size_t)pos * 40);
+#pragma unroll
+            for (int t = 0; t < 4; ++t) {
+                float4 r;
+                r.x = sa * A0[4*t+0] * cs; r.y = sa * A0[4*t+1] * cs;
+                r.z = sa * A0[4*t+2] * cs; r.w = sa * A0[4*t+3] * cs;
+                vp[t] = r;
+            }
+        }
+    }
+
+    __syncthreads();
     for (int idx = tid; idx < 4 * 256; idx += BS) {
-        const int p = idx >> 8;
+        const int pg = idx >> 8;
         const int local = idx & 255;
         const float* s0;
         const float* s1;
         if (local < 128) {
             const int j = local >> 2, rr = local & 3, ip = rr >> 1, h = rr & 1;
-            const int i0 = 4*p + 2*ip;
+            const int i0 = 4*pg + 2*ip;
             s0 = fcv_w2 + j*640 + 384 + i0*8 + 4*h;
             s1 = s0 + 8;
         } else {
             const int l = local - 128;
             const int jp = l >> 3, rr = l & 7, il = rr >> 2, h2c = rr & 3;
-            const int i = 2*p + il, j0 = 2*jp;
+            const int i = 2*pg + il, j0 = 2*jp;
             const int base = (h2c < 2) ? 512 : 576;
             s0 = fcv_w2 + j0*640 + base + i*8 + (h2c & 1)*4;
             s1 = s0 + 640;
         }
-        sb4[p * 257 + local] = make_uint4(
+        swz[pg * 257 + local] = make_uint4(
             pk2h(s0[0], s1[0]), pk2h(s0[1], s1[1]),
             pk2h(s0[2], s1[2]), pk2h(s0[3], s1[3]));
     }
-
-    const int lane = tid & 63;
-    const int p = lane >> 4;
-    const int q = lane & 15;
-    const int w = tid >> 6;
-    const int e = blockIdx.x * EPB + w * 16 + q;
-    const bool val = (e < E);
-    const int ec = val ? e : (E - 1);
-
-    const int is64 = *flag;
-    const int snd = is64 ? ei[2*ec] : ei[ec];
-
-    const float4 s4 = *(const float4*)(edge_sh + (size_t)ec * 4);
-    const float sh_s = s4.x;
-    const float sh_v[3] = {s4.y, s4.z, s4.w};
-
-    const float* nf = node_ft + (size_t)snd * 40;
-
     __syncthreads();
 
-    float hv[32];
     {
-        float es[16];
-        const float4* a0 = (const float4*)(edge_scalars + (size_t)ec * 16);
-#pragma unroll
-        for (int t = 0; t < 4; ++t) {
-            const float4 v = a0[t];
-            es[4*t+0]=v.x; es[4*t+1]=v.y; es[4*t+2]=v.z; es[4*t+3]=v.w;
-        }
-#pragma unroll 8
+        const uint4* g = swz + p * 257;
+
+        const h2 xs01 = pkrtz(nf[4*p + 0], nf[4*p + 1]);
+        const h2 xs23 = pkrtz(nf[4*p + 2], nf[4*p + 3]);
+
+        h2 T3[8] = {};
+#pragma unroll 4
         for (int j = 0; j < 32; ++j) {
-            float a = 0.f;
-#pragma unroll
-            for (int t = 0; t < 16; ++t) a += es[t] * fcv_w1[t*32 + j];
-            hv[j] = silu_f(a * 0.25f);
-        }
-    }
-
-    const uint4* g = sb4 + p * 257;
-
-    const h2 xs01 = pkrtz(nf[4*p + 0], nf[4*p + 1]);
-    const h2 xs23 = pkrtz(nf[4*p + 2], nf[4*p + 3]);
-
-    h2 T3[8] = {};
-#pragma unroll 4
-    for (int j = 0; j < 32; ++j) {
-        const uint4 E0 = g[j*4+0], E1 = g[j*4+1];
-        const uint4 F0 = g[j*4+2], F1 = g[j*4+3];
-        const h2 hh = pkrtz(hv[j], hv[j]);
-        const h2 t01 = hh * xs01, t23 = hh * xs23;
-        T3[0]=pfma(t01,uh2(E0.x),T3[0]); T3[0]=pfma(t23,uh2(F0.x),T3[0]);
-        T3[1]=pfma(t01,uh2(E0.y),T3[1]); T3[1]=pfma(t23,uh2(F0.y),T3[1]);
-        T3[2]=pfma(t01,uh2(E0.z),T3[2]); T3[2]=pfma(t23,uh2(F0.z),T3[2]);
-        T3[3]=pfma(t01,uh2(E0.w),T3[3]); T3[3]=pfma(t23,uh2(F0.w),T3[3]);
-        T3[4]=pfma(t01,uh2(E1.x),T3[4]); T3[4]=pfma(t23,uh2(F1.x),T3[4]);
-        T3[5]=pfma(t01,uh2(E1.y),T3[5]); T3[5]=pfma(t23,uh2(F1.y),T3[5]);
-        T3[6]=pfma(t01,uh2(E1.z),T3[6]); T3[6]=pfma(t23,uh2(F1.z),T3[6]);
-        T3[7]=pfma(t01,uh2(E1.w),T3[7]); T3[7]=pfma(t23,uh2(F1.w),T3[7]);
-    }
-
-    h2 P4[16] = {}, P5[16] = {};
+            const uint4 E0 = g[j*4+0], E1 = g[j*4+1];
+            const uint4 F0 = g[j*4+2], F1 = g[j*4+3];
+            const h2 hh = pkrtz(hv[j], hv[j]);
+            const h2 t01 = hh * xs01, t23 = hh * xs23;
+            T3[0]=pfma(t01,uh2(E0.x),T3[0]); T3[0]=pfma(t23,uh2(F0.x),T3[0]);
+            T3[1]=pfma(t01,uh2(E0.y),T3[1]); T3[1]=pfma(t23,uh2(F0.y),T3[1]);
+            T3[2]=pfma(t01,uh2(E0.z),T3[2]); T3[2]=pfma(t23,uh2(F0.z),T3[2]);
+            T3[3]=pfma(t01,uh2(E0.w),T3[3]); T3[3]=pfma(t23,uh2(F0.w),T3[3]);
+            T3[4]=pfma(t01,uh2(E1.x),T3[4]); T3[4]=pfma(t23,uh2(F1.x),T3[4]);
+            T3[5]=pfma(t01,uh2(E1.y),T3[5]); T3[5]=pfma(t23,uh2(F1.y),T3[5]);
+            T3[6]=pfma(t01,uh2(E1.z),T3[6]); T3[6]=pfma(t23,uh2(F1.z),T3[6]);
+            T3[7]=pfma(t01,uh2(E1.w),T3[7]); T3[7]=pfma(t23,uh2(F1.w),T3[7]);
+        }
+
+        h2 P4[16] = {}, P5[16] = {};
 #pragma unroll 2
-    for (int jp = 0; jp < 16; ++jp) {
-        const uint4* gw = g + 128 + jp*8;
-        const uint4 a4 = gw[0], b4 = gw[1];
-        const uint4 c4 = gw[2], d4 = gw[3];
-        const uint4 e4 = gw[4], f4 = gw[5];
-        const uint4 m4 = gw[6], n4 = gw[7];
-        const h2 hp = pkrtz(hv[2*jp], hv[2*jp+1]);
-        P4[0] =pfma(hp,uh2(a4.x),P4[0]);  P4[1] =pfma(hp,uh2(a4.y),P4[1]);
-        P4[2] =pfma(hp,uh2(a4.z),P4[2]);  P4[3] =pfma(hp,uh2(a4.w),P4[3]);
-        P4[4] =pfma(hp,uh2(b4.x),P4[4]);  P4[5] =pfma(hp,uh2(b4.y),P4[5]);
-        P4[6] =pfma(hp,uh2(b4.z),P4[6]);  P4[7] =pfma(hp,uh2(b4.w),P4[7]);
-        P5[0] =pfma(hp,uh2(c4.x),P5[0]);  P5[1] =pfma(hp,uh2(c4.y),P5[1]);
-        P5[2] =pfma(hp,uh2(c4.z),P5[2]);  P5[3] =pfma(hp,uh2(c4.w),P5[3]);
-        P5[4] =pfma(hp,uh2(d4.x),P5[4]);  P5[5] =pfma(hp,uh2(d4.y),P5[5]);
-        P5[6] =pfma(hp,uh2(d4.z),P5[6]);  P5[7] =pfma(hp,uh2(d4.w),P5[7]);
-        P4[8] =pfma(hp,uh2(e4.x),P4[8]);  P4[9] =pfma(hp,uh2(e4.y),P4[9]);
-        P4[10]=pfma(hp,uh2(e4.z),P4[10]); P4[11]=pfma(hp,uh2(e4.w),P4[11]);
-        P4[12]=pfma(hp,uh2(f4.x),P4[12]); P4[13]=pfma(hp,uh2(f4.y),P4[13]);
-        P4[14]=pfma(hp,uh2(f4.z),P4[14]); P4[15]=pfma(hp,uh2(f4.w),P4[15]);
-        P5[8] =pfma(hp,uh2(m4.x),P5[8]);  P5[9] =pfma(hp,uh2(m4.y),P5[9]);
-        P5[10]=pfma(hp,uh2(m4.z),P5[10]); P5[11]=pfma(hp,uh2(m4.w),P5[11]);
-        P5[12]=pfma(hp,uh2(n4.x),P5[12]); P5[13]=pfma(hp,uh2(n4.y),P5[13]);
-        P5[14]=pfma(hp,uh2(n4.z),P5[14]); P5[15]=pfma(hp,uh2(n4.w),P5[15]);
-    }
-
-    const float c7 = 0.70710678118654752f;
-    float R[24], T3f[8];
-    {
-        float acc[24];
-#pragma unroll
-        for (int o = 0; o < 24; ++o) acc[o] = 0.f;
+        for (int jp = 0; jp < 16; ++jp) {
+            const uint4* gw = g + 128 + jp*8;
+            const uint4 a4 = gw[0], b4 = gw[1];
+            const uint4 c4 = gw[2], d4 = gw[3];
+            const uint4 e4 = gw[4], f4 = gw[5];
+            const uint4 m4 = gw[6], n4 = gw[7];
+            const h2 hp = pkrtz(hv[2*jp], hv[2*jp+1]);
+            P4[0] =pfma(hp,uh2(a4.x),P4[0]);  P4[1] =pfma(hp,uh2(a4.y),P4[1]);
+            P4[2] =pfma(hp,uh2(a4.z),P4[2]);  P4[3] =pfma(hp,uh2(a4.w),P4[3]);
+            P4[4] =pfma(hp,uh2(b4.x),P4[4]);  P4[5] =pfma(hp,uh2(b4.y),P4[5]);
+            P4[6] =pfma(hp,uh2(b4.z),P4[6]);  P4[7] =pfma(hp,uh2(b4.w),P4[7]);
+            P5[0] =pfma(hp,uh2(c4.x),P5[0]);  P5[1] =pfma(hp,uh2(c4.y),P5[1]);
+            P5[2] =pfma(hp,uh2(c4.z),P5[2]);  P5[3] =pfma(hp,uh2(c4.w),P5[3]);
+            P5[4] =pfma(hp,uh2(d4.x),P5[4]);  P5[5] =pfma(hp,uh2(d4.y),P5[5]);
+            P5[6] =pfma(hp,uh2(d4.z),P5[6]);  P5[7] =pfma(hp,uh2(d4.w),P5[7]);
+            P4[8] =pfma(hp,uh2(e4.x),P4[8]);  P4[9] =pfma(hp,uh2(e4.y),P4[9]);
+            P4[10]=pfma(hp,uh2(e4.z),P4[10]); P4[11]=pfma(hp,uh2(e4.w),P4[11]);
+            P4[12]=pfma(hp,uh2(f4.x),P4[12]); P4[13]=pfma(hp,uh2(f4.y),P4[13]);
+            P4[14]=pfma(hp,uh2(f4.z),P4[14]); P4[15]=pfma(hp,uh2(f4.w),P4[15]);
+            P5[8] =pfma(hp,uh2(m4.x),P5[8]);  P5[9] =pfma(hp,uh2(m4.y),P5[9]);
+            P5[10]=pfma(hp,uh2(m4.z),P5[10]); P5[11]=pfma(hp,uh2(m4.w),P5[11]);
+            P5[12]=pfma(hp,uh2(n4.x),P5[12]); P5[13]=pfma(hp,uh2(n4.y),P5[13]);
+            P5[14]=pfma(hp,uh2(n4.z),P5[14]); P5[15]=pfma(hp,uh2(n4.w),P5[15]);
+        }
+
+        float R[24], T3f[8];
         {
-            const float x0 = nf[16 + 6*p], x1 = nf[17 + 6*p], x2 = nf[18 + 6*p];
-            const float s0 = sh_s*x0, s1 = sh_s*x1, s2 = sh_s*x2;
-            const float cx0 = c7*(x1*sh_v[2] - x2*sh_v[1]);
-            const float cx1 = c7*(x2*sh_v[0] - x0*sh_v[2]);
-            const float cx2 = c7*(x0*sh_v[1] - x1*sh_v[0]);
-#pragma unroll
-            for (int o = 0; o < 8; ++o) {
-                const float w4 = h2s(P4[o]), w5 = h2s(P5[o]);
-                acc[o*3+0] += s0*w4 + cx0*w5;
-                acc[o*3+1] += s1*w4 + cx1*w5;
-                acc[o*3+2] += s2*w4 + cx2*w5;
-            }
-        }
-        {
-            const float x0 = nf[19 + 6*p], x1 = nf[20 + 6*p], x2 = nf[21 + 6*p];
-            const float s0 = sh_s*x0, s1 = sh_s*x1, s2 = sh_s*x2;
-            const float cx0 = c7*(x1*sh_v[2] - x2*sh_v[1]);
-            const float cx1 = c7*(x2*sh_v[0] - x0*sh_v[2]);
-            const float cx2 = c7*(x0*sh_v[1] - x1*sh_v[0]);
-#pragma unroll
-            for (int o = 0; o < 8; ++o) {
-                const float w4 = h2s(P4[8+o]), w5 = h2s(P5[8+o]);
-                acc[o*3+0] += s0*w4 + cx0*w5;
-                acc[o*3+1] += s1*w4 + cx1*w5;
-                acc[o*3+2] += s2*w4 + cx2*w5;
-            }
-        }
-#pragma unroll
-        for (int o = 0; o < 24; ++o) R[o] = wred4(acc[o]);
-    }
-#pragma unroll
-    for (int o = 0; o < 8; ++o) T3f[o] = wred4(h2s(T3[o]));
-
-    if (p == 0 && val) {
-        const float sc = 0.03125f;
-        const float sa = sabuf[e];
-        const int pos = posbuf[e];
-        float row[24];
-#pragma unroll
-        for (int o = 0; o < 8; ++o)
-#pragma unroll
-            for (int c = 0; c < 3; ++c)
-                row[o*3+c] = sa * (T3f[o]*sh_v[c] + R[o*3+c]) * sc;
-        float4* vp = (float4*)(vbuf + (size_t)pos * 40 + 16);
-#pragma unroll
-        for (int t = 0; t < 6; ++t) {
-            float4 r; r.x = row[4*t+0]; r.y = row[4*t+1]; r.z = row[4*t+2]; r.w = row[4*t+3];
-            vp[t] = r;
+            float acc[24];
+#pragma unroll
+            for (int o = 0; o < 24; ++o) acc[o] = 0.f;
+            {
+                const float x0 = nf[16 + 6*p], x1 = nf[17 + 6*p], x2 = nf[18 + 6*p];
+                const float s0 = sh_s*x0, s1 = sh_s*x1, s2 = sh_s*x2;
+                const float cx0 = c7*(x1*sh_v[2] - x2*sh_v[1]);
+                const float cx1 = c7*(x2*sh_v[0] - x0*sh_v[2]);
+                const float cx2 = c7*(x0*sh_v[1] - x1*sh_v[0]);
+#pragma unroll
+                for (int o = 0; o < 8; ++o) {
+                    const float w4 = h2s(P4[o]), w5 = h2s(P5[o]);
+                    acc[o*3+0] += s0*w4 + cx0*w5;
+                    acc[o*3+1] += s1*w4 + cx1*w5;
+                    acc[o*3+2] += s2*w4 + cx2*w5;
+                }
+            }
+            {
+                const float x0 = nf[19 + 6*p], x1 = nf[20 + 6*p], x2 = nf[21 + 6*p];
+                const float s0 = sh_s*x0, s1 = sh_s*x1, s2 = sh_s*x2;
+                const float cx0 = c7*(x1*sh_v[2] - x2*sh_v[1]);
+                const float cx1 = c7*(x2*sh_v[0] - x0*sh_v[2]);
+                const float cx2 = c7*(x0*sh_v[1] - x1*sh_v[0]);
+#pragma unroll
+                for (int o = 0; o < 8; ++o) {
+                    const float w4 = h2s(P4[8+o]), w5 = h2s(P5[8+o]);
+                    acc[o*3+0] += s0*w4 + cx0*w5;
+                    acc[o*3+1] += s1*w4 + cx1*w5;
+                    acc[o*3+2] += s2*w4 + cx2*w5;
+                }
+            }
+#pragma unroll
+            for (int o = 0; o < 24; ++o) R[o] = wred4(acc[o]);
+        }
+#pragma unroll
+        for (int o = 0; o < 8; ++o) T3f[o] = wred4(h2s(T3[o]));
+
+        if (p == 0 && val) {
+            const float sc = 0.03125f;
+            float row[24];
+#pragma unroll
+            for (int o = 0; o < 8; ++o)
+#pragma unroll
+                for (int c = 0; c < 3; ++c)
+                    row[o*3+c] = sa * (T3f[o]*sh_v[c] + R[o*3+c]) * sc;
+            float4* vp = (float4*)(vbuf + (size_t)pos * 40 + 16);
+#pragma unroll
+            for (int t = 0; t < 6; ++t) {
+                float4 r; r.x = row[4*t+0]; r.y = row[4*t+1]; r.z = row[4*t+2]; r.w = row[4*t+3];
+                vp[t] = r;
+            }
         }
     }
 }
@@ -720,30 +626,23 @@
     size_t off   = (size_t)N * 20 + N + (N + 1) + N + 1;
     off = (off + 3) & ~(size_t)3;
     float* exbuf  = ws + off;
-    float* sabuf  = exbuf + E;
-    int*   posbuf = (int*)(sabuf + E);
-    float* vbuf   = (float*)(posbuf + E);
+    float* vbuf   = exbuf + E;
 
     float* out = (float*)d_out;
 
+    const int NE = (E > N) ? E : N;
     const int EB = (E + EPB - 1) / EPB;
 
-    hipLaunchKernelGGL(node_pre, dim3((N + 255) / 256), dim3(256), 0, stream,
+    hipMemsetAsync(cnt, 0, (size_t)N * sizeof(int), stream);
+    hipLaunchKernelGGL(pre_count, dim3((NE + 255) / 256), dim3(256), 0, stream,
                        node_ft, edge_index, w_q_s, w_q_v, wdot_s, wdot_v,
                        qd, cnt, flg, N, E);
-    hipLaunchKernelGGL(count_edges, dim3((E + 255) / 256), dim3(256), 0, stream,
-                       edge_index, cnt, flg, E);
     hipLaunchKernelGGL(scan_kernel, dim3(1), dim3(1024), 0, stream,
                        cnt, start, curs, N);
-    hipLaunchKernelGGL(edge_k, dim3(EB), dim3(BS), 0, stream,
+    hipLaunchKernelGGL(edge_all, dim3(EB), dim3(BS), 0, stream,
                        node_ft, edge_index, edge_sh, edge_scalars,
-                       fck_w1, fck_w2, qd, curs, exbuf, sabuf, posbuf, flg, N, E);
-    hipLaunchKernelGGL(edge_v_a, dim3(EB), dim3(BS), 0, stream,
-                       node_ft, edge_index, edge_sh, edge_scalars,
-                       fcv_w1, fcv_w2, sabuf, posbuf, vbuf, flg, E);
-    hipLaunchKernelGGL(edge_v_b, dim3(EB), dim3(BS), 0, stream,
-                       node_ft, edge_index, edge_sh, edge_scalars,
-                       fcv_w1, fcv_w2, sabuf, posbuf, vbuf, flg, E);
+                       fck_w1, fck_w2, fcv_w1, fcv_w2,
+                       qd, curs, exbuf, vbuf, flg, N, E);
     hipLaunchKernelGGL(node_reduce, dim3((N + 3) / 4), dim3(256), 0, stream,
                        start, exbuf, vbuf, out, N);
 }
```

New measurement: 269.1 us. Within noise of the previous version (-0.0%).
